# Performance work log

Hardware: AMD Instinct MI355X
Metric: run time of the kernel (lower is better)

Reference implementation:

```python
import jax, jax.numpy as jnp
import numpy as np

BN, BE, B = 50000, 800000, 16
NE, EE, GE, EH, NH = 32, 32, 32, 128, 128  # emb dims, hidden dims


def clean(x):
    return jnp.nan_to_num(x, nan=0.0, posinf=0.0, neginf=0.0)


def _lin(key, fan_in, fan_out):
    k1, k2 = jax.random.split(key)
    s = 1.0 / np.sqrt(fan_in)
    return (jax.random.uniform(k1, (fan_in, fan_out), jnp.float32, -s, s),
            jax.random.uniform(k2, (fan_out,), jnp.float32, -s, s))


def setup_inputs() -> dict:
    key = jax.random.key(0)
    ks = jax.random.split(key, 20)
    inp = {
        "x": jax.random.normal(ks[0], (BN, 2), jnp.float32),
        "edge_index": jax.random.randint(ks[1], (2, BE), 0, BN, jnp.int32),
        "batch": jax.random.randint(ks[2], (BN,), 0, B, jnp.int32),
        "node_attr": jnp.ones((BN, 2), jnp.float32),
        "edge_attr": jax.random.uniform(ks[3], (BE, 2), jnp.float32) + 0.5,  # positive spacings
        "glob_attr": jax.random.uniform(ks[4], (B, 2), jnp.float32),
    }
    # encoders (output 2*emb each, 'Duplicated')
    inp["enc_node_W"], inp["enc_node_b"] = _lin(ks[5], 2, 2 * NE)
    inp["enc_edge_W"], inp["enc_edge_b"] = _lin(ks[6], 2, 2 * EE)
    inp["enc_glob_W"], inp["enc_glob_b"] = _lin(ks[7], 2, 2 * GE)
    inp["enc2_W"], inp["enc2_b"] = _lin(ks[8], 2, 2 * EE)
    # derivative MLP: 4*NE+2*EE -> EH -> 2*EE
    inp["dW1"], inp["db1"] = _lin(ks[9], 4 * NE + 2 * EE, EH)
    inp["dW2"], inp["db2"] = _lin(ks[10], EH, 2 * EE)
    # half-jacobian MLP: 4*EE -> EH -> 2*EE
    inp["hW1"], inp["hb1"] = _lin(ks[11], 4 * EE, EH)
    inp["hW2"], inp["hb2"] = _lin(ks[12], EH, 2 * EE)
    # jacobian MLP: 6*EE -> NH -> 2*NE
    inp["jW1"], inp["jb1"] = _lin(ks[13], 6 * EE, NH)
    inp["jW2"], inp["jb2"] = _lin(ks[14], NH, 2 * NE)
    # hessian MLP: 4*EE+2*EE -> NH -> 2*NE
    inp["sW1"], inp["sb1"] = _lin(ks[15], 6 * EE, NH)
    inp["sW2"], inp["sb2"] = _lin(ks[16], NH, 2 * NE)
    # node MLP: 6*NE+2*GE -> NH -> 2*NE
    inp["nW1"], inp["nb1"] = _lin(ks[17], 6 * NE + 2 * GE, NH)
    inp["nW2"], inp["nb2"] = _lin(ks[18], NH, 2 * NE)
    # decoder: 2*NE -> 2
    inp["decW"], inp["decb"] = _lin(ks[19], 2 * NE, 2)
    return inp


def reference(x, edge_index, batch, node_attr, edge_attr, glob_attr,
              enc_node_W, enc_node_b, enc_edge_W, enc_edge_b, enc_glob_W, enc_glob_b,
              enc2_W, enc2_b,
              dW1, db1, dW2, db2,
              hW1, hb1, hW2, hb2,
              jW1, jb1, jW2, jb2,
              sW1, sb1, sW2, sb2,
              nW1, nb1, nW2, nb2,
              decW, decb):
    relu = jax.nn.relu
    seg = lambda d, idx: jax.ops.segment_sum(d, idx, num_segments=BN)
    mlp = lambda t, W1, b1, W2, b2: relu(t @ W1 + b1) @ W2 + b2

    row, col = edge_index[0], edge_index[1]
    spacing = edge_attr                                 # [BE,2]
    inv_spacing = clean(1.0 / spacing)
    inv_double = clean(1.0 / (seg(spacing, row) + seg(spacing, col)))  # [BN,2]

    node_emb = relu(x @ enc_node_W + enc_node_b)        # [BN,2*NE]
    spacing_emb = relu(spacing @ enc_edge_W + enc_edge_b)  # [BE,2*EE]
    glob_emb = relu(glob_attr @ enc_glob_W + enc_glob_b)   # [B,2*GE]
    inv_spacing_emb = relu(inv_spacing @ enc2_W + enc2_b)  # [BE,2*EE]
    inv_double_emb = relu(inv_double @ enc2_W + enc2_b)    # [BN,2*EE]

    d_edge = mlp(jnp.concatenate([node_emb[row], node_emb[col], inv_spacing_emb], -1),
                 dW1, db1, dW2, db2)                    # [BE,2*EE]
    hj_plus = seg(d_edge, row)                          # [BN,2*EE]
    hj_minus = seg(d_edge, col)

    jac1 = seg(mlp(jnp.concatenate([spacing_emb, hj_plus[col]], -1), hW1, hb1, hW2, hb2), col)
    jac2 = seg(mlp(jnp.concatenate([spacing_emb, hj_minus[row]], -1), hW1, hb1, hW2, hb2), row)
    jac = mlp(jnp.concatenate([jac1, jac2, inv_double_emb], -1), jW1, jb1, jW2, jb2)  # [BN,2*NE]

    hess = mlp(jnp.concatenate([hj_plus, hj_minus, inv_double_emb], -1), sW1, sb1, sW2, sb2)

    res = mlp(jnp.concatenate([node_emb, jac, glob_emb[batch], hess], -1), nW1, nb1, nW2, nb2)
    return node_attr * (res @ decW + decb)              # [BN,2]
```

## Files before the change

### kernel.cpp

```cpp
#include <hip/hip_runtime.h>
#include <math.h>

#define BN 50000
#define BE 800000

__device__ __forceinline__ float relu_f(float v) { return fmaxf(v, 0.0f); }
__device__ __forceinline__ float inv_clean(float s) {
    float q = 1.0f / s;
    return isfinite(q) ? q : 0.0f;
}
__device__ __forceinline__ float inv_clean_fast(float s) {
    float q = __builtin_amdgcn_rcpf(s);
    return isfinite(q) ? q : 0.0f;
}

__global__ __launch_bounds__(256) void k_pack_w1(
    const float* __restrict__ W, int r0, float4* __restrict__ dst)
{
    int t = blockIdx.x * 256 + threadIdx.x;
    if (t >= 2048) return;
    int j2 = t >> 6, l = t & 63;
    const float* ra = W + (size_t)(r0 + 2*j2) * 128 + 2*l;
    const float* rb = W + (size_t)(r0 + 2*j2 + 1) * 128 + 2*l;
    dst[t] = make_float4(ra[0], ra[1], rb[0], rb[1]);
}
__global__ __launch_bounds__(256) void k_pack_w2(
    const float* __restrict__ W2, float4* __restrict__ dst)
{
    int t = blockIdx.x * 256 + threadIdx.x;
    if (t >= 2048) return;
    int k4 = t >> 6, l = t & 63;
    dst[t] = make_float4(W2[(4*k4+0)*64+l], W2[(4*k4+1)*64+l],
                         W2[(4*k4+2)*64+l], W2[(4*k4+3)*64+l]);
}
__global__ __launch_bounds__(256) void k_pack_uv(
    const float* __restrict__ dW1, float4* __restrict__ dst)
{
    int t = blockIdx.x * 256 + threadIdx.x;
    if (t >= 4096) return;
    int j = t >> 6, l = t & 63;
    float4 w;
    if (l < 32) w = ((const float4*)(dW1 + (size_t)j*128))[l];
    else        w = ((const float4*)(dW1 + (size_t)(64+j)*128))[l-32];
    dst[t] = w;
}

__global__ __launch_bounds__(256) void k_node_enc(
    const float* __restrict__ x, const float* __restrict__ W,
    const float* __restrict__ b, float* __restrict__ node_emb)
{
    int t = blockIdx.x * 256 + threadIdx.x;
    int i = t >> 6, l = t & 63;
    float v = fmaf(x[i*2], W[l], fmaf(x[i*2+1], W[64+l], b[l]));
    node_emb[t] = relu_f(v);
}


__global__ __launch_bounds__(256, 6) void k_uv(
    const float* __restrict__ ne, const float4* __restrict__ guv,
    float* __restrict__ u, float* __restrict__ v)
{
    extern __shared__ float lds[];
    const int wid = threadIdx.x >> 6, l = threadIdx.x & 63;
    float4* xb4 = (float4*)(lds + wid * 512);
    const int gw = blockIdx.x * 4 + wid;
    const int nw = gridDim.x * 4;

    for (int g = gw; g < BN/8; g += nw) {
        const int n0 = g * 8;
        const int q = l >> 5;
        #pragma unroll
        for (int r = 0; r < 2; r++) {
            int j = (l & 31) + 32*r;
            float v0 = ne[(n0 + q*4 + 0)*64 + j];
            float v1 = ne[(n0 + q*4 + 1)*64 + j];
            float v2 = ne[(n0 + q*4 + 2)*64 + j];
            float v3 = ne[(n0 + q*4 + 3)*64 + j];
            xb4[j*2 + q] = make_float4(v0, v1, v2, v3);
        }
        float4 acc[8];
        #pragma unroll
        for (int e = 0; e < 8; e++) acc[e] = make_float4(0,0,0,0);
        #pragma unroll 8
        for (int j = 0; j < 64; j++) {
            float4 wq = guv[j*64 + l];
            float4 xa = xb4[j*2 + 0];
            float4 xc = xb4[j*2 + 1];
            acc[0].x = fmaf(xa.x, wq.x, acc[0].x); acc[0].y = fmaf(xa.x, wq.y, acc[0].y);
            acc[0].z = fmaf(xa.x, wq.z, acc[0].z); acc[0].w = fmaf(xa.x, wq.w, acc[0].w);
            acc[1].x = fmaf(xa.y, wq.x, acc[1].x); acc[1].y = fmaf(xa.y, wq.y, acc[1].y);
            acc[1].z = fmaf(xa.y, wq.z, acc[1].z); acc[1].w = fmaf(xa.y, wq.w, acc[1].w);
            acc[2].x = fmaf(xa.z, wq.x, acc[2].x); acc[2].y = fmaf(xa.z, wq.y, acc[2].y);
            acc[2].z = fmaf(xa.z, wq.z, acc[2].z); acc[2].w = fmaf(xa.z, wq.w, acc[2].w);
            acc[3].x = fmaf(xa.w, wq.x, acc[3].x); acc[3].y = fmaf(xa.w, wq.y, acc[3].y);
            acc[3].z = fmaf(xa.w, wq.z, acc[3].z); acc[3].w = fmaf(xa.w, wq.w, acc[3].w);
            acc[4].x = fmaf(xc.x, wq.x, acc[4].x); acc[4].y = fmaf(xc.x, wq.y, acc[4].y);
            acc[4].z = fmaf(xc.x, wq.z, acc[4].z); acc[4].w = fmaf(xc.x, wq.w, acc[4].w);
            acc[5].x = fmaf(xc.y, wq.x, acc[5].x); acc[5].y = fmaf(xc.y, wq.y, acc[5].y);
            acc[5].z = fmaf(xc.y, wq.z, acc[5].z); acc[5].w = fmaf(xc.y, wq.w, acc[5].w);
            acc[6].x = fmaf(xc.z, wq.x, acc[6].x); acc[6].y = fmaf(xc.z, wq.y, acc[6].y);
            acc[6].z = fmaf(xc.z, wq.z, acc[6].z); acc[6].w = fmaf(xc.z, wq.w, acc[6].w);
            acc[7].x = fmaf(xc.w, wq.x, acc[7].x); acc[7].y = fmaf(xc.w, wq.y, acc[7].y);
            acc[7].z = fmaf(xc.w, wq.z, acc[7].z); acc[7].w = fmaf(xc.w, wq.w, acc[7].w);
        }
        float* dst = (l < 32) ? (u + 4*l) : (v + 4*(l-32));
        #pragma unroll
        for (int e = 0; e < 8; e++) {
            *(float4*)(dst + (size_t)(n0+e)*128) = acc[e];
        }
    }
}

__global__ __launch_bounds__(256, 6) void k_tptm(
    const float* __restrict__ hjp, const float* __restrict__ hjm,
    const float4* __restrict__ gtp,
    float* __restrict__ tp, float* __restrict__ tm)
{
    extern __shared__ float lds[];
    const int wid = threadIdx.x >> 6, l = threadIdx.x & 63;
    float4* xb4 = (float4*)(lds + wid * 512);
    const int gw = blockIdx.x * 4 + wid;
    const int nw = gridDim.x * 4;
    const int NG = BN/8;

    for (int vg = gw; vg < 2*NG; vg += nw) {
        const float* in  = (vg < NG) ? hjp : hjm;
        float*       out = (vg < NG) ? tp  : tm;
        const int n0 = ((vg < NG) ? vg : vg - NG) * 8;
        const int q = l >> 5;
        #pragma unroll
        for (int r = 0; r < 2; r++) {
            int j = (l & 31) + 32*r;
            float v0 = in[(n0 + q*4 + 0)*64 + j];
            float v1 = in[(n0 + q*4 + 1)*64 + j];
            float v2 = in[(n0 + q*4 + 2)*64 + j];
            float v3 = in[(n0 + q*4 + 3)*64 + j];
            xb4[j*2 + q] = make_float4(v0, v1, v2, v3);
        }
        float a0[8] = {0,0,0,0,0,0,0,0}, a1[8] = {0,0,0,0,0,0,0,0};
        #pragma unroll 8
        for (int j2 = 0; j2 < 32; j2++) {
            float4 wq = gtp[j2*64 + l];
            float4 xa = xb4[(2*j2)*2 + 0];
            float4 xbv = xb4[(2*j2)*2 + 1];
            float4 xc = xb4[(2*j2+1)*2 + 0];
            float4 xd = xb4[(2*j2+1)*2 + 1];
            a0[0] = fmaf(xa.x, wq.x, fmaf(xc.x, wq.z, a0[0]));
            a1[0] = fmaf(xa.x, wq.y, fmaf(xc.x, wq.w, a1[0]));
            a0[1] = fmaf(xa.y, wq.x, fmaf(xc.y, wq.z, a0[1]));
            a1[1] = fmaf(xa.y, wq.y, fmaf(xc.y, wq.w, a1[1]));
            a0[2] = fmaf(xa.z, wq.x, fmaf(xc.z, wq.z, a0[2]));
            a1[2] = fmaf(xa.z, wq.y, fmaf(xc.z, wq.w, a1[2]));
            a0[3] = fmaf(xa.w, wq.x, fmaf(xc.w, wq.z, a0[3]));
            a1[3] = fmaf(xa.w, wq.y, fmaf(xc.w, wq.w, a1[3]));
            a0[4] = fmaf(xbv.x, wq.x, fmaf(xd.x, wq.z, a0[4]));
            a1[4] = fmaf(xbv.x, wq.y, fmaf(xd.x, wq.w, a1[4]));
            a0[5] = fmaf(xbv.y, wq.x, fmaf(xd.y, wq.z, a0[5]));
            a1[5] = fmaf(xbv.y, wq.y, fmaf(xd.y, wq.w, a1[5]));
            a0[6] = fmaf(xbv.z, wq.x, fmaf(xd.z, wq.z, a0[6]));
            a1[6] = fmaf(xbv.z, wq.y, fmaf(xd.z, wq.w, a1[6]));
            a0[7] = fmaf(xbv.w, wq.x, fmaf(xd.w, wq.z, a0[7]));
            a1[7] = fmaf(xbv.w, wq.y, fmaf(xd.w, wq.w, a1[7]));
        }
        #pragma unroll
        for (int e = 0; e < 8; e++) {
            *(float2*)(out + (size_t)(n0+e)*128 + 2*l) = make_float2(a0[e], a1[e]);
        }
    }
}

__global__ __launch_bounds__(256, 6) void k_edge1f(
    const int* __restrict__ ei, const float* __restrict__ ea,
    const float* __restrict__ u, const float* __restrict__ v,
    const float* __restrict__ e2w, const float* __restrict__ e2b,
    const float4* __restrict__ gw1, const float* __restrict__ db1,
    const float4* __restrict__ gw2, const float* __restrict__ db2,
    float* __restrict__ sumsp, float* __restrict__ hjp, float* __restrict__ hjm)
{
    extern __shared__ float lds[];
    const int wid = threadIdx.x >> 6, l = threadIdx.x & 63;
    float* buf = lds + wid * 1024;
    float4* buf4 = (float4*)buf;

    const int jA = l >> 1;
    const int eh = l & 1;
    const float ewA0 = e2w[jA],      ewB0 = e2w[64+jA],    eb0v = e2b[jA];
    const float ewA1 = e2w[jA+32],   ewB1 = e2w[96+jA],    eb1v = e2b[jA+32];
    const float b1a = db1[2*l], b1b = db1[2*l+1];
    const float b2r = db2[l];

    const int gw = blockIdx.x * 4 + wid;
    const int nw = gridDim.x * 4;

    for (int g = gw; g < BE/8; g += nw) {
        const int e0 = g * 8;
        int4 r01 = *(const int4*)(ei + e0);
        int4 r2  = *(const int4*)(ei + e0 + 4);
        int4 c01 = *(const int4*)(ei + BE + e0);
        int4 c2  = *(const int4*)(ei + BE + e0 + 4);
        float4 sv0 = ((const float4*)(ea + 2*e0))[0];
        float4 sv1 = ((const float4*)(ea + 2*e0))[1];
        float4 sv2 = ((const float4*)(ea + 2*e0))[2];
        float4 sv3 = ((const float4*)(ea + 2*e0))[3];

        if (l < 32) {
            int e = l >> 2, wch = l & 3;
            int4 rA = (e & 4) ? r2 : r01;
            int rx = (e & 2) ? ((e & 1) ? rA.w : rA.z) : ((e & 1) ? rA.y : rA.x);
            int4 cA = (e & 4) ? c2 : c01;
            int cx = (e & 2) ? ((e & 1) ? cA.w : cA.z) : ((e & 1) ? cA.y : cA.x);
            float4 sA = (e & 4) ? ((e & 2) ? sv3 : sv2) : ((e & 2) ? sv1 : sv0);
            float s0e = (e & 1) ? sA.z : sA.x;
            float s1e = (e & 1) ? sA.w : sA.y;
            int node = (wch < 2) ? rx : cx;
            int comp = wch & 1;
            float val = comp ? s1e : s0e;
            atomicAdd(&sumsp[node*2 + comp], val);
        }

        {
            float4 svA = eh ? sv2 : sv0;
            float4 svB = eh ? sv3 : sv1;
            float q00 = inv_clean_fast(svA.x), q10 = inv_clean_fast(svA.y);
            float q01 = inv_clean_fast(svA.z), q11 = inv_clean_fast(svA.w);
            float q02 = inv_clean_fast(svB.x), q12 = inv_clean_fast(svB.y);
            float q03 = inv_clean_fast(svB.z), q13 = inv_clean_fast(svB.w);
            float4 p0, p1;
            p0.x = relu_f(fmaf(q00, ewA0, fmaf(q10, ewB0, eb0v)));
            p0.y = relu_f(fmaf(q01, ewA0, fmaf(q11, ewB0, eb0v)));
            p0.z = relu_f(fmaf(q02, ewA0, fmaf(q12, ewB0, eb0v)));
            p0.w = relu_f(fmaf(q03, ewA0, fmaf(q13, ewB0, eb0v)));
            p1.x = relu_f(fmaf(q00, ewA1, fmaf(q10, ewB1, eb1v)));
            p1.y = relu_f(fmaf(q01, ewA1, fmaf(q11, ewB1, eb1v)));
            p1.z = relu_f(fmaf(q02, ewA1, fmaf(q12, ewB1, eb1v)));
            p1.w = relu_f(fmaf(q03, ewA1, fmaf(q13, ewB1, eb1v)));
            buf4[jA*2 + eh]      = p0;
            buf4[(jA+32)*2 + eh] = p1;
        }

        float t0[8], t1[8];
        {
            const int rr[8] = {r01.x, r01.y, r01.z, r01.w, r2.x, r2.y, r2.z, r2.w};
            const int cc[8] = {c01.x, c01.y, c01.z, c01.w, c2.x, c2.y, c2.z, c2.w};
            #pragma unroll
            for (int e = 0; e < 8; e++) {
                float2 uu = *(const float2*)(u + (size_t)rr[e]*128 + 2*l);
                float2 vv = *(const float2*)(v + (size_t)cc[e]*128 + 2*l);
                t0[e] = b1a + uu.x + vv.x;
                t1[e] = b1b + uu.y + vv.y;
            }
        }

        #pragma unroll 8
        for (int j2 = 0; j2 < 32; j2++) {
            float4 wq = gw1[j2*64 + l];
            float4 xa = buf4[(2*j2)*2 + 0];
            float4 xbv = buf4[(2*j2)*2 + 1];
            float4 xc = buf4[(2*j2+1)*2 + 0];
            float4 xd = buf4[(2*j2+1)*2 + 1];
            t0[0] = fmaf(xa.x, wq.x, fmaf(xc.x, wq.z, t0[0]));
            t1[0] = fmaf(xa.x, wq.y, fmaf(xc.x, wq.w, t1[0]));
            t0[1] = fmaf(xa.y, wq.x, fmaf(xc.y, wq.z, t0[1]));
            t1[1] = fmaf(xa.y, wq.y, fmaf(xc.y, wq.w, t1[1]));
            t0[2] = fmaf(xa.z, wq.x, fmaf(xc.z, wq.z, t0[2]));
            t1[2] = fmaf(xa.z, wq.y, fmaf(xc.z, wq.w, t1[2]));
            t0[3] = fmaf(xa.w, wq.x, fmaf(xc.w, wq.z, t0[3]));
            t1[3] = fmaf(xa.w, wq.y, fmaf(xc.w, wq.w, t1[3]));
            t0[4] = fmaf(xbv.x, wq.x, fmaf(xd.x, wq.z, t0[4]));
            t1[4] = fmaf(xbv.x, wq.y, fmaf(xd.x, wq.w, t1[4]));
            t0[5] = fmaf(xbv.y, wq.x, fmaf(xd.y, wq.z, t0[5]));
            t1[5] = fmaf(xbv.y, wq.y, fmaf(xd.y, wq.w, t1[5]));
            t0[6] = fmaf(xbv.z, wq.x, fmaf(xd.z, wq.z, t0[6]));
            t1[6] = fmaf(xbv.z, wq.y, fmaf(xd.z, wq.w, t1[6]));
            t0[7] = fmaf(xbv.w, wq.x, fmaf(xd.w, wq.z, t0[7]));
            t1[7] = fmaf(xbv.w, wq.y, fmaf(xd.w, wq.w, t1[7]));
        }

        #pragma unroll
        for (int e = 0; e < 8; e++) {
            *(float2*)(buf + e*128 + 2*l) = make_float2(relu_f(t0[e]), relu_f(t1[e]));
        }
        float o[8] = {0,0,0,0,0,0,0,0};
        #pragma unroll 8
        for (int k4 = 0; k4 < 32; k4++) {
            float4 wq = gw2[k4*64 + l];
            #pragma unroll
            for (int e = 0; e < 8; e++) {
                float4 hb = *(const float4*)(buf + e*128 + 4*k4);
                o[e] = fmaf(hb.x, wq.x, fmaf(hb.y, wq.y,
                        fmaf(hb.z, wq.z, fmaf(hb.w, wq.w, o[e]))));
            }
        }
        {
            const int rr[8] = {r01.x, r01.y, r01.z, r01.w, r2.x, r2.y, r2.z, r2.w};
            const int cc[8] = {c01.x, c01.y, c01.z, c01.w, c2.x, c2.y, c2.z, c2.w};
            #pragma unroll
            for (int e = 0; e < 8; e++) {
                float ov = o[e] + b2r;
                atomicAdd(&hjp[(size_t)rr[e]*64 + l], ov);
                atomicAdd(&hjm[(size_t)cc[e]*64 + l], ov);
            }
        }
    }
}

__global__ __launch_bounds__(256, 6) void k_edge2f(
    const int* __restrict__ ei, const float* __restrict__ ea,
    const float* __restrict__ tp, const float* __restrict__ tm,
    const float* __restrict__ eew, const float* __restrict__ eeb,
    const float4* __restrict__ gw1, const float* __restrict__ hb1,
    const float4* __restrict__ gw2, const float* __restrict__ hb2,
    float* __restrict__ jac1, float* __restrict__ jac2)
{
    extern __shared__ float lds[];
    const int wid = threadIdx.x >> 6, l = threadIdx.x & 63;
    float* buf = lds + wid * 1024;
    float4* buf4 = (float4*)buf;

    const int jA = l >> 1;
    const int eh = l & 1;
    const float ewA0 = eew[jA],    ewB0 = eew[64+jA],  eb0v = eeb[jA];
    const float ewA1 = eew[jA+32], ewB1 = eew[96+jA],  eb1v = eeb[jA+32];
    const float b1a = hb1[2*l], b1b = hb1[2*l+1];
    const float b2r = hb2[l];

    const int gw = blockIdx.x * 4 + wid;
    const int nw = gridDim.x * 4;

    for (int g = gw; g < BE/8; g += nw) {
        const int e0 = g * 8;
        int4 r01 = *(const int4*)(ei + e0);
        int4 r2  = *(const int4*)(ei + e0 + 4);
        int4 c01 = *(const int4*)(ei + BE + e0);
        int4 c2  = *(const int4*)(ei + BE + e0 + 4);
        float4 sv0 = ((const float4*)(ea + 2*e0))[0];
        float4 sv1 = ((const float4*)(ea + 2*e0))[1];
        float4 sv2 = ((const float4*)(ea + 2*e0))[2];
        float4 sv3 = ((const float4*)(ea + 2*e0))[3];

        {
            float4 svA = eh ? sv2 : sv0;
            float4 svB = eh ? sv3 : sv1;
            float4 p0, p1;
            p0.x = relu_f(fmaf(svA.x, ewA0, fmaf(svA.y, ewB0, eb0v)));
            p0.y = relu_f(fmaf(svA.z, ewA0, fmaf(svA.w, ewB0, eb0v)));
            p0.z = relu_f(fmaf(svB.x, ewA0, fmaf(svB.y, ewB0, eb0v)));
            p0.w = relu_f(fmaf(svB.z, ewA0, fmaf(svB.w, ewB0, eb0v)));
            p1.x = relu_f(fmaf(svA.x, ewA1, fmaf(svA.y, ewB1, eb1v)));
            p1.y = relu_f(fmaf(svA.z, ewA1, fmaf(svA.w, ewB1, eb1v)));
            p1.z = relu_f(fmaf(svB.x, ewA1, fmaf(svB.y, ewB1, eb1v)));
            p1.w = relu_f(fmaf(svB.z, ewA1, fmaf(svB.w, ewB1, eb1v)));
            buf4[jA*2 + eh]      = p0;
            buf4[(jA+32)*2 + eh] = p1;
        }

        const int rr[8] = {r01.x, r01.y, r01.z, r01.w, r2.x, r2.y, r2.z, r2.w};
        const int cc[8] = {c01.x, c01.y, c01.z, c01.w, c2.x, c2.y, c2.z, c2.w};

        float2 tpv[8];
        #pragma unroll
        for (int e = 0; e < 8; e++)
            tpv[e] = *(const float2*)(tp + (size_t)cc[e]*128 + 2*l);

        float t0[8], t1[8];
        #pragma unroll
        for (int e = 0; e < 8; e++) { t0[e] = b1a; t1[e] = b1b; }

        #pragma unroll 8
        for (int j2 = 0; j2 < 32; j2++) {
            float4 wq = gw1[j2*64 + l];
            float4 xa = buf4[(2*j2)*2 + 0];
            float4 xbv = buf4[(2*j2)*2 + 1];
            float4 xc = buf4[(2*j2+1)*2 + 0];
            float4 xd = buf4[(2*j2+1)*2 + 1];
            t0[0] = fmaf(xa.x, wq.x, fmaf(xc.x, wq.z, t0[0]));
            t1[0] = fmaf(xa.x, wq.y, fmaf(xc.x, wq.w, t1[0]));
            t0[1] = fmaf(xa.y, wq.x, fmaf(xc.y, wq.z, t0[1]));
            t1[1] = fmaf(xa.y, wq.y, fmaf(xc.y, wq.w, t1[1]));
            t0[2] = fmaf(xa.z, wq.x, fmaf(xc.z, wq.z, t0[2]));
            t1[2] = fmaf(xa.z, wq.y, fmaf(xc.z, wq.w, t1[2]));
            t0[3] = fmaf(xa.w, wq.x, fmaf(xc.w, wq.z, t0[3]));
            t1[3] = fmaf(xa.w, wq.y, fmaf(xc.w, wq.w, t1[3]));
            t0[4] = fmaf(xbv.x, wq.x, fmaf(xd.x, wq.z, t0[4]));
            t1[4] = fmaf(xbv.x, wq.y, fmaf(xd.x, wq.w, t1[4]));
            t0[5] = fmaf(xbv.y, wq.x, fmaf(xd.y, wq.z, t0[5]));
            t1[5] = fmaf(xbv.y, wq.y, fmaf(xd.y, wq.w, t1[5]));
            t0[6] = fmaf(xbv.z, wq.x, fmaf(xd.z, wq.z, t0[6]));
            t1[6] = fmaf(xbv.z, wq.y, fmaf(xd.z, wq.w, t1[6]));
            t0[7] = fmaf(xbv.w, wq.x, fmaf(xd.w, wq.z, t0[7]));
            t1[7] = fmaf(xbv.w, wq.y, fmaf(xd.w, wq.w, t1[7]));
        }

        #pragma unroll
        for (int e = 0; e < 8; e++) {
            *(float2*)(buf + e*128 + 2*l) =
                make_float2(relu_f(t0[e] + tpv[e].x), relu_f(t1[e] + tpv[e].y));
        }
        float2 tmv[8];
        #pragma unroll
        for (int e = 0; e < 8; e++)
            tmv[e] = *(const float2*)(tm + (size_t)rr[e]*128 + 2*l);

        float o1[8] = {0,0,0,0,0,0,0,0};
        #pragma unroll 8
        for (int k4 = 0; k4 < 32; k4++) {
            float4 wq = gw2[k4*64 + l];
            #pragma unroll
            for (int e = 0; e < 8; e++) {
                float4 hb = *(const float4*)(buf + e*128 + 4*k4);
                o1[e] = fmaf(hb.x, wq.x, fmaf(hb.y, wq.y,
                         fmaf(hb.z, wq.z, fmaf(hb.w, wq.w, o1[e]))));
            }
        }
        #pragma unroll
        for (int e = 0; e < 8; e++)
            atomicAdd(&jac1[(size_t)cc[e]*64 + l], o1[e] + b2r);

        #pragma unroll
        for (int e = 0; e < 8; e++) {
            *(float2*)(buf + e*128 + 2*l) =
                make_float2(relu_f(t0[e] + tmv[e].x), relu_f(t1[e] + tmv[e].y));
        }
        float o2[8] = {0,0,0,0,0,0,0,0};
        #pragma unroll 8
        for (int k4 = 0; k4 < 32; k4++) {
            float4 wq = gw2[k4*64 + l];
            #pragma unroll
            for (int e = 0; e < 8; e++) {
                float4 hb = *(const float4*)(buf + e*128 + 4*k4);
                o2[e] = fmaf(hb.x, wq.x, fmaf(hb.y, wq.y,
                         fmaf(hb.z, wq.z, fmaf(hb.w, wq.w, o2[e]))));
            }
        }
        #pragma unroll
        for (int e = 0; e < 8; e++)
            atomicAdd(&jac2[(size_t)rr[e]*64 + l], o2[e] + b2r);
    }
}

__global__ __launch_bounds__(256, 4) void k_node_mlp(
    const float* __restrict__ A, const float* __restrict__ Bv,
    const float* __restrict__ sumsp,
    const float* __restrict__ e2w_g, const float* __restrict__ e2b_g,
    const float* __restrict__ W1g, const float* __restrict__ b1g,
    const float* __restrict__ W2g, const float* __restrict__ b2g,
    float* __restrict__ outp)
{
    extern __shared__ float lds[];
    const int wid = threadIdx.x >> 6, l = threadIdx.x & 63;
    float* xbuf = lds + wid * 768;
    float* hbuf = lds + 4*768 + wid * 512;

    const float ewl = e2w_g[l], ewl2 = e2w_g[64+l], ebl = e2b_g[l];
    const float bb0 = b1g[2*l], bb1 = b1g[2*l+1];
    const float bo = b2g[l];

    const int gw = blockIdx.x * 4 + wid;
    const int nw = gridDim.x * 4;

    for (int g = gw; g < BN/4; g += nw) {
        const int i0 = g * 4;
        float av[4], bv[4], iv[4];
        #pragma unroll
        for (int e = 0; e < 4; e++) {
            int i = i0 + e;
            av[e] = A[i*64 + l];
            bv[e] = Bv[i*64 + l];
            float q0 = inv_clean(sumsp[i*2+0]);
            float q1 = inv_clean(sumsp[i*2+1]);
            iv[e] = relu_f(fmaf(q0, ewl, fmaf(q1, ewl2, ebl)));
        }
        ((float4*)xbuf)[l]       = make_float4(av[0], av[1], av[2], av[3]);
        ((float4*)xbuf)[64 + l]  = make_float4(bv[0], bv[1], bv[2], bv[3]);
        ((float4*)xbuf)[128 + l] = make_float4(iv[0], iv[1], iv[2], iv[3]);

        float acc0[4] = {0,0,0,0}, acc1[4] = {0,0,0,0};
        #pragma unroll 8
        for (int j = 0; j < 192; j++) {
            float4 xv = ((const float4*)xbuf)[j];
            float2 wv = ((const float2*)(W1g + j*128))[l];
            acc0[0] = fmaf(xv.x, wv.x, acc0[0]);
            acc0[1] = fmaf(xv.y, wv.x, acc0[1]);
            acc0[2] = fmaf(xv.z, wv.x, acc0[2]);
            acc0[3] = fmaf(xv.w, wv.x, acc0[3]);
            acc1[0] = fmaf(xv.x, wv.y, acc1[0]);
            acc1[1] = fmaf(xv.y, wv.y, acc1[1]);
            acc1[2] = fmaf(xv.z, wv.y, acc1[2]);
            acc1[3] = fmaf(xv.w, wv.y, acc1[3]);
        }
        #pragma unroll
        for (int e = 0; e < 4; e++) {
            ((float2*)(hbuf + e*128))[l] = make_float2(relu_f(acc0[e]+bb0), relu_f(acc1[e]+bb1));
        }
        float o[4] = {0,0,0,0};
        #pragma unroll 8
        for (int k = 0; k < 128; k++) {
            float wv = W2g[k*64 + l];
            o[0] = fmaf(hbuf[0*128+k], wv, o[0]);
            o[1] = fmaf(hbuf[1*128+k], wv, o[1]);
            o[2] = fmaf(hbuf[2*128+k], wv, o[2]);
            o[3] = fmaf(hbuf[3*128+k], wv, o[3]);
        }
        #pragma unroll
        for (int e = 0; e < 4; e++) outp[(i0+e)*64 + l] = o[e] + bo;
    }
}

__global__ __launch_bounds__(256, 4) void k_node_final(
    const float* __restrict__ node_emb, const float* __restrict__ jacv,
    const float* __restrict__ hessv,
    const int* __restrict__ batch, const float* __restrict__ ga,
    const float* __restrict__ gw_g, const float* __restrict__ gb_g,
    const float* __restrict__ nW1, const float* __restrict__ nb1,
    const float* __restrict__ nW2, const float* __restrict__ nb2,
    const float* __restrict__ decW, const float* __restrict__ decb,
    const float* __restrict__ node_attr, float* __restrict__ outp)
{
    extern __shared__ float lds[];
    const int wid = threadIdx.x >> 6, l = threadIdx.x & 63;
    float* xbuf = lds + wid * 1024;
    float* hbuf = lds + 4*1024 + wid * 512;

    const float gwl = gw_g[l], gwl2 = gw_g[64+l], gbl = gb_g[l];
    const float bb0 = nb1[2*l], bb1 = nb1[2*l+1];
    const float bo = nb2[l];

    const int gwv = blockIdx.x * 4 + wid;
    const int nw = gridDim.x * 4;

    for (int g = gwv; g < BN/4; g += nw) {
        const int i0 = g * 4;
        float ne[4], jv[4], ge[4], hv[4];
        #pragma unroll
        for (int e = 0; e < 4; e++) {
            int i = i0 + e;
            ne[e] = node_emb[i*64 + l];
            jv[e] = jacv[i*64 + l];
            hv[e] = hessv[i*64 + l];
            int gi = batch[i];
            ge[e] = relu_f(fmaf(ga[gi*2], gwl, fmaf(ga[gi*2+1], gwl2, gbl)));
        }
        ((float4*)xbuf)[l]       = make_float4(ne[0], ne[1], ne[2], ne[3]);
        ((float4*)xbuf)[64 + l]  = make_float4(jv[0], jv[1], jv[2], jv[3]);
        ((float4*)xbuf)[128 + l] = make_float4(ge[0], ge[1], ge[2], ge[3]);
        ((float4*)xbuf)[192 + l] = make_float4(hv[0], hv[1], hv[2], hv[3]);

        float acc0[4] = {0,0,0,0}, acc1[4] = {0,0,0,0};
        #pragma unroll 8
        for (int j = 0; j < 256; j++) {
            float4 xv = ((const float4*)xbuf)[j];
            float2 wv = ((const float2*)(nW1 + j*128))[l];
            acc0[0] = fmaf(xv.x, wv.x, acc0[0]);
            acc0[1] = fmaf(xv.y, wv.x, acc0[1]);
            acc0[2] = fmaf(xv.z, wv.x, acc0[2]);
            acc0[3] = fmaf(xv.w, wv.x, acc0[3]);
            acc1[0] = fmaf(xv.x, wv.y, acc1[0]);
            acc1[1] = fmaf(xv.y, wv.y, acc1[1]);
            acc1[2] = fmaf(xv.z, wv.y, acc1[2]);
            acc1[3] = fmaf(xv.w, wv.y, acc1[3]);
        }
        #pragma unroll
        for (int e = 0; e < 4; e++) {
            ((float2*)(hbuf + e*128))[l] = make_float2(relu_f(acc0[e]+bb0), relu_f(acc1[e]+bb1));
        }
        float o[4] = {0,0,0,0};
        #pragma unroll 8
        for (int k = 0; k < 128; k++) {
            float wv = nW2[k*64 + l];
            o[0] = fmaf(hbuf[0*128+k], wv, o[0]);
            o[1] = fmaf(hbuf[1*128+k], wv, o[1]);
            o[2] = fmaf(hbuf[2*128+k], wv, o[2]);
            o[3] = fmaf(hbuf[3*128+k], wv, o[3]);
        }
        #pragma unroll
        for (int e = 0; e < 4; e++) hbuf[e*128 + l] = o[e] + bo;

        int e2 = l >> 4, sub = l & 15, j2 = sub >> 3, part = sub & 7;
        float s = 0.0f;
        #pragma unroll
        for (int kk = 0; kk < 8; kk++) {
            int k = part*8 + kk;
            s = fmaf(hbuf[e2*128 + k], decW[k*2 + j2], s);
        }
        s += __shfl_xor(s, 1);
        s += __shfl_xor(s, 2);
        s += __shfl_xor(s, 4);
        if (part == 0) {
            int i = i0 + e2;
            outp[i*2 + j2] = (s + decb[j2]) * node_attr[i*2 + j2];
        }
    }
}

__global__ __launch_bounds__(256) void k_edge1(
    const int* __restrict__ ei, const float* __restrict__ ea,
    const float* __restrict__ node_emb,
    const float* __restrict__ e2w_g, const float* __restrict__ e2b_g,
    const float* __restrict__ dW1, const float* __restrict__ db1,
    const float* __restrict__ dW2, const float* __restrict__ db2,
    float* __restrict__ sumsp, float* __restrict__ hjp, float* __restrict__ hjm)
{
    extern __shared__ float lds[];
    float* w1 = lds;
    float* b1 = w1 + 192*128;
    float* w2 = b1 + 128;
    float* b2 = w2 + 128*64;
    float* ew = b2 + 64;
    float* eb = ew + 128;
    float* xreg = eb + 64;
    float* hreg = xreg + 4*768;

    for (int idx = threadIdx.x; idx < 192*128; idx += 256) w1[idx] = dW1[idx];
    for (int idx = threadIdx.x; idx < 128*64; idx += 256)  w2[idx] = dW2[idx];
    if (threadIdx.x < 128) { b1[threadIdx.x] = db1[threadIdx.x]; ew[threadIdx.x] = e2w_g[threadIdx.x]; }
    if (threadIdx.x < 64)  { b2[threadIdx.x] = db2[threadIdx.x]; eb[threadIdx.x] = e2b_g[threadIdx.x]; }
    __syncthreads();

    const int wid = threadIdx.x >> 6, l = threadIdx.x & 63;
    float* xbuf = xreg + wid * 768;
    float* hbuf = hreg + wid * 512;
    const int gw = blockIdx.x * 4 + wid;
    const int nw = gridDim.x * 4;

    for (int g = gw; g < BE/4; g += nw) {
        const int e0 = g * 4;
        int r[4], c[4];
        float s0[4], s1[4];
        #pragma unroll
        for (int e = 0; e < 4; e++) {
            r[e]  = ei[e0+e];
            c[e]  = ei[BE + e0+e];
            s0[e] = ea[(e0+e)*2+0];
            s1[e] = ea[(e0+e)*2+1];
        }
        if (l < 16) {
            int e = l >> 2, wch = l & 3;
            int node = (wch < 2) ? r[e] : c[e];
            float v = (wch & 1) ? s1[e] : s0[e];
            atomicAdd(&sumsp[node*2 + (wch & 1)], v);
        }
        float ar[4], cr[4], ir[4];
        #pragma unroll
        for (int e = 0; e < 4; e++) {
            ar[e] = node_emb[r[e]*64 + l];
            cr[e] = node_emb[c[e]*64 + l];
            float q0 = inv_clean(s0[e]), q1 = inv_clean(s1[e]);
            ir[e] = relu_f(fmaf(q0, ew[l], fmaf(q1, ew[64+l], eb[l])));
        }
        ((float4*)xbuf)[l]       = make_float4(ar[0], ar[1], ar[2], ar[3]);
        ((float4*)xbuf)[64 + l]  = make_float4(cr[0], cr[1], cr[2], cr[3]);
        ((float4*)xbuf)[128 + l] = make_float4(ir[0], ir[1], ir[2], ir[3]);

        float acc0[4] = {0,0,0,0}, acc1[4] = {0,0,0,0};
        #pragma unroll 8
        for (int j = 0; j < 192; j++) {
            float4 xv = ((const float4*)xbuf)[j];
            float2 wv = ((const float2*)(w1 + j*128))[l];
            acc0[0] = fmaf(xv.x, wv.x, acc0[0]);
            acc0[1] = fmaf(xv.y, wv.x, acc0[1]);
            acc0[2] = fmaf(xv.z, wv.x, acc0[2]);
            acc0[3] = fmaf(xv.w, wv.x, acc0[3]);
            acc1[0] = fmaf(xv.x, wv.y, acc1[0]);
            acc1[1] = fmaf(xv.y, wv.y, acc1[1]);
            acc1[2] = fmaf(xv.z, wv.y, acc1[2]);
            acc1[3] = fmaf(xv.w, wv.y, acc1[3]);
        }
        float bb0 = b1[2*l], bb1 = b1[2*l+1];
        #pragma unroll
        for (int e = 0; e < 4; e++) {
            float2 h = make_float2(relu_f(acc0[e]+bb0), relu_f(acc1[e]+bb1));
            ((float2*)(hbuf + e*128))[l] = h;
        }
        float o[4] = {0,0,0,0};
        #pragma unroll 8
        for (int k = 0; k < 128; k++) {
            float wv = w2[k*64 + l];
            o[0] = fmaf(hbuf[0*128+k], wv, o[0]);
            o[1] = fmaf(hbuf[1*128+k], wv, o[1]);
            o[2] = fmaf(hbuf[2*128+k], wv, o[2]);
            o[3] = fmaf(hbuf[3*128+k], wv, o[3]);
        }
        float bo = b2[l];
        #pragma unroll
        for (int e = 0; e < 4; e++) {
            float ov = o[e] + bo;
            atomicAdd(&hjp[r[e]*64 + l], ov);
            atomicAdd(&hjm[c[e]*64 + l], ov);
        }
    }
}

__global__ __launch_bounds__(256) void k_edge2(
    const int* __restrict__ ei, const float* __restrict__ ea,
    const float* __restrict__ hjp, const float* __restrict__ hjm,
    const float* __restrict__ eew_g, const float* __restrict__ eeb_g,
    const float* __restrict__ hW1, const float* __restrict__ hb1,
    const float* __restrict__ hW2, const float* __restrict__ hb2,
    float* __restrict__ jac1, float* __restrict__ jac2)
{
    extern __shared__ float lds[];
    float* w1 = lds;
    float* b1 = w1 + 128*128;
    float* w2 = b1 + 128;
    float* b2 = w2 + 128*64;
    float* ew = b2 + 64;
    float* eb = ew + 128;
    float* base = eb + 64;

    for (int idx = threadIdx.x; idx < 128*128; idx += 256) w1[idx] = hW1[idx];
    for (int idx = threadIdx.x; idx < 128*64; idx += 256)  w2[idx] = hW2[idx];
    if (threadIdx.x < 128) { b1[threadIdx.x] = hb1[threadIdx.x]; ew[threadIdx.x] = eew_g[threadIdx.x]; }
    if (threadIdx.x < 64)  { b2[threadIdx.x] = hb2[threadIdx.x]; eb[threadIdx.x] = eeb_g[threadIdx.x]; }
    __syncthreads();

    const int wid = threadIdx.x >> 6, l = threadIdx.x & 63;
    float* x1 = base + wid*2048;
    float* x2 = x1 + 512;
    float* h1 = x2 + 512;
    float* h2 = h1 + 512;
    const int gw = blockIdx.x * 4 + wid;
    const int nw = gridDim.x * 4;

    for (int g = gw; g < BE/4; g += nw) {
        const int e0 = g * 4;
        int r[4], c[4];
        float se[4], pa[4], pb[4];
        #pragma unroll
        for (int e = 0; e < 4; e++) {
            r[e] = ei[e0+e];
            c[e] = ei[BE + e0+e];
            float sp0 = ea[(e0+e)*2+0], sp1 = ea[(e0+e)*2+1];
            se[e] = relu_f(fmaf(sp0, ew[l], fmaf(sp1, ew[64+l], eb[l])));
            pa[e] = hjp[c[e]*64 + l];
            pb[e] = hjm[r[e]*64 + l];
        }
        ((float4*)x1)[l]      = make_float4(se[0], se[1], se[2], se[3]);
        ((float4*)x1)[64 + l] = make_float4(pa[0], pa[1], pa[2], pa[3]);
        ((float4*)x2)[l]      = make_float4(se[0], se[1], se[2], se[3]);
        ((float4*)x2)[64 + l] = make_float4(pb[0], pb[1], pb[2], pb[3]);

        float a0[4]={0,0,0,0}, a1[4]={0,0,0,0}, b0v[4]={0,0,0,0}, b1v[4]={0,0,0,0};
        #pragma unroll 8
        for (int j = 0; j < 128; j++) {
            float2 wv = ((const float2*)(w1 + j*128))[l];
            float4 xa = ((const float4*)x1)[j];
            float4 xb = ((const float4*)x2)[j];
            a0[0]=fmaf(xa.x,wv.x,a0[0]); a0[1]=fmaf(xa.y,wv.x,a0[1]);
            a0[2]=fmaf(xa.z,wv.x,a0[2]); a0[3]=fmaf(xa.w,wv.x,a0[3]);
            a1[0]=fmaf(xa.x,wv.y,a1[0]); a1[1]=fmaf(xa.y,wv.y,a1[1]);
            a1[2]=fmaf(xa.z,wv.y,a1[2]); a1[3]=fmaf(xa.w,wv.y,a1[3]);
            b0v[0]=fmaf(xb.x,wv.x,b0v[0]); b0v[1]=fmaf(xb.y,wv.x,b0v[1]);
            b0v[2]=fmaf(xb.z,wv.x,b0v[2]); b0v[3]=fmaf(xb.w,wv.x,b0v[3]);
            b1v[0]=fmaf(xb.x,wv.y,b1v[0]); b1v[1]=fmaf(xb.y,wv.y,b1v[1]);
            b1v[2]=fmaf(xb.z,wv.y,b1v[2]); b1v[3]=fmaf(xb.w,wv.y,b1v[3]);
        }
        float bb0 = b1[2*l], bb1 = b1[2*l+1];
        #pragma unroll
        for (int e = 0; e < 4; e++) {
            ((float2*)(h1 + e*128))[l] = make_float2(relu_f(a0[e]+bb0), relu_f(a1[e]+bb1));
            ((float2*)(h2 + e*128))[l] = make_float2(relu_f(b0v[e]+bb0), relu_f(b1v[e]+bb1));
        }
        float oA[4]={0,0,0,0}, oB[4]={0,0,0,0};
        #pragma unroll 8
        for (int k = 0; k < 128; k++) {
            float wv = w2[k*64 + l];
            oA[0]=fmaf(h1[0*128+k],wv,oA[0]); oA[1]=fmaf(h1[1*128+k],wv,oA[1]);
            oA[2]=fmaf(h1[2*128+k],wv,oA[2]); oA[3]=fmaf(h1[3*128+k],wv,oA[3]);
            oB[0]=fmaf(h2[0*128+k],wv,oB[0]); oB[1]=fmaf(h2[1*128+k],wv,oB[1]);
            oB[2]=fmaf(h2[2*128+k],wv,oB[2]); oB[3]=fmaf(h2[3*128+k],wv,oB[3]);
        }
        float bo = b2[l];
        #pragma unroll
        for (int e = 0; e < 4; e++) {
            atomicAdd(&jac1[c[e]*64 + l], oA[e] + bo);
            atomicAdd(&jac2[r[e]*64 + l], oB[e] + bo);
        }
    }
}

extern "C" void kernel_launch(void* const* d_in, const int* in_sizes, int n_in,
                              void* d_out, int out_size, void* d_ws, size_t ws_size,
                              hipStream_t stream) {
    const float* x          = (const float*)d_in[0];
    const int*   ei         = (const int*)  d_in[1];
    const int*   batch      = (const int*)  d_in[2];
    const float* node_attr  = (const float*)d_in[3];
    const float* edge_attr  = (const float*)d_in[4];
    const float* glob_attr  = (const float*)d_in[5];
    const float* enc_node_W = (const float*)d_in[6];
    const float* enc_node_b = (const float*)d_in[7];
    const float* enc_edge_W = (const float*)d_in[8];
    const float* enc_edge_b = (const float*)d_in[9];
    const float* enc_glob_W = (const float*)d_in[10];
    const float* enc_glob_b = (const float*)d_in[11];
    const float* enc2_W     = (const float*)d_in[12];
    const float* enc2_b     = (const float*)d_in[13];
    const float* dW1 = (const float*)d_in[14]; const float* db1 = (const float*)d_in[15];
    const float* dW2 = (const float*)d_in[16]; const float* db2 = (const float*)d_in[17];
    const float* hW1 = (const float*)d_in[18]; const float* hb1 = (const float*)d_in[19];
    const float* hW2 = (const float*)d_in[20]; const float* hb2 = (const float*)d_in[21];
    const float* jW1 = (const float*)d_in[22]; const float* jb1 = (const float*)d_in[23];
    const float* jW2 = (const float*)d_in[24]; const float* jb2 = (const float*)d_in[25];
    const float* sW1 = (const float*)d_in[26]; const float* sb1 = (const float*)d_in[27];
    const float* sW2 = (const float*)d_in[28]; const float* sb2 = (const float*)d_in[29];
    const float* nW1 = (const float*)d_in[30]; const float* nb1 = (const float*)d_in[31];
    const float* nW2 = (const float*)d_in[32]; const float* nb2 = (const float*)d_in[33];
    const float* decW = (const float*)d_in[34]; const float* decb = (const float*)d_in[35];

    float* ws = (float*)d_ws;
    const size_t NEED_FAST = 28900000ull * sizeof(float);

    if (ws_size >= NEED_FAST) {
        float* ne    = ws;
        float* u     = ne + 3200000;
        float* v     = u + 6400000;
        float* hjp   = v + 6400000;
        float* hjm   = hjp + 3200000;
        float* jac1  = hjm + 3200000;
        float* jac2  = jac1 + 3200000;
        float* sumsp = jac2 + 3200000;

        float* scratch = (float*)d_out;
        float4* puv   = (float4*)(scratch);
        float4* pw1e1 = (float4*)(scratch + 16384);
        float4* pw2e1 = (float4*)(scratch + 24576);
        float4* pw1tp = (float4*)(scratch + 32768);
        float4* pw1e2 = (float4*)(scratch + 40960);
        float4* pw2e2 = (float4*)(scratch + 49152);

        hipMemsetAsync(hjp, 0, (size_t)4*3200000*sizeof(float), stream);
        hipMemsetAsync(sumsp, 0, (size_t)100000*sizeof(float), stream);

        k_pack_uv<<<16, 256, 0, stream>>>(dW1, puv);
        k_pack_w1<<<8, 256, 0, stream>>>(dW1, 128, pw1e1);
        k_pack_w2<<<8, 256, 0, stream>>>(dW2, pw2e1);
        k_pack_w1<<<8, 256, 0, stream>>>(hW1, 64, pw1tp);
        k_pack_w1<<<8, 256, 0, stream>>>(hW1, 0, pw1e2);
        k_pack_w2<<<8, 256, 0, stream>>>(hW2, pw2e2);

        k_node_enc<<<12500, 256, 0, stream>>>(x, enc_node_W, enc_node_b, ne);

        k_uv<<<1536, 256, 2048*4, stream>>>(ne, puv, u, v);

        k_edge1f<<<1536, 256, 4096*4, stream>>>(ei, edge_attr, u, v, enc2_W, enc2_b,
                                                pw1e1, db1, pw2e1, db2, sumsp, hjp, hjm);

        k_tptm<<<1536, 256, 2048*4, stream>>>(hjp, hjm, pw1tp, u, v);

        k_edge2f<<<1536, 256, 4096*4, stream>>>(ei, edge_attr, u, v,
                                                enc_edge_W, enc_edge_b,
                                                pw1e2, hb1, pw2e2, hb2, jac1, jac2);

        size_t lds_nm = (4*768 + 4*512) * sizeof(float);
        k_node_mlp<<<1024, 256, lds_nm, stream>>>(jac1, jac2, sumsp, enc2_W, enc2_b,
                                                  jW1, jb1, jW2, jb2, jac1);
        k_node_mlp<<<1024, 256, lds_nm, stream>>>(hjp, hjm, sumsp, enc2_W, enc2_b,
                                                  sW1, sb1, sW2, sb2, hjp);

        size_t lds_nf = (4*1024 + 4*512) * sizeof(float);
        k_node_final<<<1024, 256, lds_nf, stream>>>(ne, jac1, hjp,
                                                    batch, glob_attr, enc_glob_W, enc_glob_b,
                                                    nW1, nb1, nW2, nb2, decW, decb,
                                                    node_attr, (float*)d_out);
    } else {
        float* node_emb = ws;
        float* hjp   = node_emb + 3200000;
        float* hjm   = hjp + 3200000;
        float* jac1  = hjm + 3200000;
        float* jac2  = jac1 + 3200000;
        float* sumsp = jac2 + 3200000;

        hipMemsetAsync(hjp, 0, (size_t)4*3200000*sizeof(float), stream);
        hipMemsetAsync(sumsp, 0, (size_t)100000*sizeof(float), stream);

        k_node_enc<<<12500, 256, 0, stream>>>(x, enc_node_W, enc_node_b, node_emb);

        size_t lds1 = 38272u * sizeof(float);
        k_edge1<<<256, 256, lds1, stream>>>(ei, edge_attr, node_emb, enc2_W, enc2_b,
                                            dW1, db1, dW2, db2, sumsp, hjp, hjm);

        size_t lds2 = 33152u * sizeof(float);
        k_edge2<<<256, 256, lds2, stream>>>(ei, edge_attr, hjp, hjm,
                                            enc_edge_W, enc_edge_b,
                                            hW1, hb1, hW2, hb2, jac1, jac2);

        size_t lds_nm = (4*768 + 4*512) * sizeof(float);
        k_node_mlp<<<1024, 256, lds_nm, stream>>>(jac1, jac2, sumsp, enc2_W, enc2_b,
                                                  jW1, jb1, jW2, jb2, jac1);
        k_node_mlp<<<1024, 256, lds_nm, stream>>>(hjp, hjm, sumsp, enc2_W, enc2_b,
                                                  sW1, sb1, sW2, sb2, hjp);

        size_t lds_nf = (4*1024 + 4*512) * sizeof(float);
        k_node_final<<<1024, 256, lds_nf, stream>>>(node_emb, jac1, hjp,
                                                    batch, glob_attr, enc_glob_W, enc_glob_b,
                                                    nW1, nb1, nW2, nb2, decW, decb,
                                                    node_attr, (float*)d_out);
    }
}
```

Measured before the change: 2.092 ms.

## Sort edges by destination via CSR and merge atomics per run

Builds CSR-style sorted edge lists for rows and columns on the device (histogram, scan, scatter), then reruns the edge MLP kernels once per direction over the sorted lists. Consecutive edges that share a destination are accumulated in registers and flushed with a single atomic, which replaces per-edge atomics and the atomic segment sum of spacings. It also recomputes node embeddings inside the final kernel, because the node-embedding buffer is reused for the CSR arrays. The cost is running the edge-1 MLP twice (once per direction) plus the gather overhead of indirect edge ids.

```diff
diff --git a/kernel.cpp b/kernel.cpp
--- a/kernel.cpp
+++ b/kernel.cpp
@@ -3,6 +3,7 @@
 
 #define BN 50000
 #define BE 800000
+#define CHUNK 200
 
 __device__ __forceinline__ float relu_f(float v) { return fmaxf(v, 0.0f); }
 __device__ __forceinline__ float inv_clean(float s) {
@@ -45,6 +46,77 @@
     dst[t] = w;
 }
 
+__global__ __launch_bounds__(256) void k_hist(
+    const int* __restrict__ ei, int* __restrict__ rc, int* __restrict__ cc)
+{
+    int e = blockIdx.x * 256 + threadIdx.x;
+    if (e >= BE) return;
+    atomicAdd(&rc[ei[e]], 1);
+    atomicAdd(&cc[ei[BE + e]], 1);
+}
+
+__global__ __launch_bounds__(1024) void k_scan(
+    const int* __restrict__ cntR, int* __restrict__ offR, int* __restrict__ hdR,
+    const int* __restrict__ cntC, int* __restrict__ offC, int* __restrict__ hdC)
+{
+    __shared__ int s[1024];
+    const int* cnt; int* off; int* hd;
+    if (blockIdx.x == 0) { cnt = cntR; off = offR; hd = hdR; }
+    else                 { cnt = cntC; off = offC; hd = hdC; }
+    int t = threadIdx.x;
+    int base = t * 49;
+    int sum = 0;
+    for (int i = 0; i < 49; i++) {
+        int idx = base + i;
+        sum += (idx < BN) ? cnt[idx] : 0;
+    }
+    s[t] = sum;
+    __syncthreads();
+    for (int o = 1; o < 1024; o <<= 1) {
+        int v = (t >= o) ? s[t - o] : 0;
+        __syncthreads();
+        s[t] += v;
+        __syncthreads();
+    }
+    int run = s[t] - sum;
+    for (int i = 0; i < 49; i++) {
+        int idx = base + i;
+        if (idx < BN) {
+            off[idx] = run;
+            hd[idx] = run;
+            run += cnt[idx];
+        }
+    }
+    if (t == 1023) off[BN] = run;
+}
+
+__global__ __launch_bounds__(256) void k_scatter(
+    const int* __restrict__ ei, int* __restrict__ rhd, int* __restrict__ chd,
+    int* __restrict__ rel, int* __restrict__ cel)
+{
+    int e = blockIdx.x * 256 + threadIdx.x;
+    if (e >= BE) return;
+    int p1 = atomicAdd(&rhd[ei[e]], 1);      rel[p1] = e;
+    int p2 = atomicAdd(&chd[ei[BE + e]], 1); cel[p2] = e;
+}
+
+__global__ __launch_bounds__(256) void k_sumsp(
+    const float* __restrict__ ea,
+    const int* __restrict__ roff, const int* __restrict__ rel,
+    const int* __restrict__ coff, const int* __restrict__ cel,
+    float* __restrict__ sumsp)
+{
+    int n = blockIdx.x * 256 + threadIdx.x;
+    if (n >= BN) return;
+    float s0 = 0.f, s1 = 0.f;
+    int e0 = roff[n], e1 = roff[n+1];
+    for (int j = e0; j < e1; j++) { int e = rel[j]; s0 += ea[2*e]; s1 += ea[2*e+1]; }
+    e0 = coff[n]; e1 = coff[n+1];
+    for (int j = e0; j < e1; j++) { int e = cel[j]; s0 += ea[2*e]; s1 += ea[2*e+1]; }
+    sumsp[2*n]   = s0;
+    sumsp[2*n+1] = s1;
+}
+
 __global__ __launch_bounds__(256) void k_node_enc(
     const float* __restrict__ x, const float* __restrict__ W,
     const float* __restrict__ b, float* __restrict__ node_emb)
@@ -54,7 +126,6 @@
     float v = fmaf(x[i*2], W[l], fmaf(x[i*2+1], W[64+l], b[l]));
     node_emb[t] = relu_f(v);
 }
-
 
 __global__ __launch_bounds__(256, 6) void k_uv(
     const float* __restrict__ ne, const float4* __restrict__ guv,
@@ -169,13 +240,14 @@
     }
 }
 
-__global__ __launch_bounds__(256, 6) void k_edge1f(
-    const int* __restrict__ ei, const float* __restrict__ ea,
+__global__ __launch_bounds__(256, 6) void k_edge1s(
+    const int* __restrict__ elist, const int* __restrict__ ei,
+    const float* __restrict__ ea,
     const float* __restrict__ u, const float* __restrict__ v,
     const float* __restrict__ e2w, const float* __restrict__ e2b,
     const float4* __restrict__ gw1, const float* __restrict__ db1,
     const float4* __restrict__ gw2, const float* __restrict__ db2,
-    float* __restrict__ sumsp, float* __restrict__ hjp, float* __restrict__ hjm)
+    int mergeRow, float* __restrict__ out)
 {
     extern __shared__ float lds[];
     const int wid = threadIdx.x >> 6, l = threadIdx.x & 63;
@@ -189,66 +261,57 @@
     const float b1a = db1[2*l], b1b = db1[2*l+1];
     const float b2r = db2[l];
 
-    const int gw = blockIdx.x * 4 + wid;
-    const int nw = gridDim.x * 4;
-
-    for (int g = gw; g < BE/8; g += nw) {
-        const int e0 = g * 8;
-        int4 r01 = *(const int4*)(ei + e0);
-        int4 r2  = *(const int4*)(ei + e0 + 4);
-        int4 c01 = *(const int4*)(ei + BE + e0);
-        int4 c2  = *(const int4*)(ei + BE + e0 + 4);
-        float4 sv0 = ((const float4*)(ea + 2*e0))[0];
-        float4 sv1 = ((const float4*)(ea + 2*e0))[1];
-        float4 sv2 = ((const float4*)(ea + 2*e0))[2];
-        float4 sv3 = ((const float4*)(ea + 2*e0))[3];
-
-        if (l < 32) {
-            int e = l >> 2, wch = l & 3;
-            int4 rA = (e & 4) ? r2 : r01;
-            int rx = (e & 2) ? ((e & 1) ? rA.w : rA.z) : ((e & 1) ? rA.y : rA.x);
-            int4 cA = (e & 4) ? c2 : c01;
-            int cx = (e & 2) ? ((e & 1) ? cA.w : cA.z) : ((e & 1) ? cA.y : cA.x);
-            float4 sA = (e & 4) ? ((e & 2) ? sv3 : sv2) : ((e & 2) ? sv1 : sv0);
-            float s0e = (e & 1) ? sA.z : sA.x;
-            float s1e = (e & 1) ? sA.w : sA.y;
-            int node = (wch < 2) ? rx : cx;
-            int comp = wch & 1;
-            float val = comp ? s1e : s0e;
-            atomicAdd(&sumsp[node*2 + comp], val);
-        }
-
+    const int wave = blockIdx.x * 4 + wid;
+    const int start = wave * CHUNK;
+    const int end = min(start + CHUNK, BE);
+
+    float acc = 0.f;
+    int cur = -1;
+
+    for (int i = start; i < end; i += 8) {
+        const int nact = min(8, end - i);
+        int eid[8], rr[8], cc[8];
+        float2 spv[8];
+        #pragma unroll
+        for (int e = 0; e < 8; e++) {
+            int idx = i + ((e < nact) ? e : nact - 1);
+            eid[e] = elist[idx];
+        }
+        #pragma unroll
+        for (int e = 0; e < 8; e++) {
+            rr[e] = ei[eid[e]];
+            cc[e] = ei[BE + eid[e]];
+            spv[e] = *(const float2*)(ea + 2*(size_t)eid[e]);
+        }
         {
-            float4 svA = eh ? sv2 : sv0;
-            float4 svB = eh ? sv3 : sv1;
-            float q00 = inv_clean_fast(svA.x), q10 = inv_clean_fast(svA.y);
-            float q01 = inv_clean_fast(svA.z), q11 = inv_clean_fast(svA.w);
-            float q02 = inv_clean_fast(svB.x), q12 = inv_clean_fast(svB.y);
-            float q03 = inv_clean_fast(svB.z), q13 = inv_clean_fast(svB.w);
+            float2 sA = eh ? spv[4] : spv[0];
+            float2 sB = eh ? spv[5] : spv[1];
+            float2 sC = eh ? spv[6] : spv[2];
+            float2 sD = eh ? spv[7] : spv[3];
+            float qA0 = inv_clean_fast(sA.x), qA1 = inv_clean_fast(sA.y);
+            float qB0 = inv_clean_fast(sB.x), qB1 = inv_clean_fast(sB.y);
+            float qC0 = inv_clean_fast(sC.x), qC1 = inv_clean_fast(sC.y);
+            float qD0 = inv_clean_fast(sD.x), qD1 = inv_clean_fast(sD.y);
             float4 p0, p1;
-            p0.x = relu_f(fmaf(q00, ewA0, fmaf(q10, ewB0, eb0v)));
-            p0.y = relu_f(fmaf(q01, ewA0, fmaf(q11, ewB0, eb0v)));
-            p0.z = relu_f(fmaf(q02, ewA0, fmaf(q12, ewB0, eb0v)));
-            p0.w = relu_f(fmaf(q03, ewA0, fmaf(q13, ewB0, eb0v)));
-            p1.x = relu_f(fmaf(q00, ewA1, fmaf(q10, ewB1, eb1v)));
-            p1.y = relu_f(fmaf(q01, ewA1, fmaf(q11, ewB1, eb1v)));
-            p1.z = relu_f(fmaf(q02, ewA1, fmaf(q12, ewB1, eb1v)));
-            p1.w = relu_f(fmaf(q03, ewA1, fmaf(q13, ewB1, eb1v)));
+            p0.x = relu_f(fmaf(qA0, ewA0, fmaf(qA1, ewB0, eb0v)));
+            p0.y = relu_f(fmaf(qB0, ewA0, fmaf(qB1, ewB0, eb0v)));
+            p0.z = relu_f(fmaf(qC0, ewA0, fmaf(qC1, ewB0, eb0v)));
+            p0.w = relu_f(fmaf(qD0, ewA0, fmaf(qD1, ewB0, eb0v)));
+            p1.x = relu_f(fmaf(qA0, ewA1, fmaf(qA1, ewB1, eb1v)));
+            p1.y = relu_f(fmaf(qB0, ewA1, fmaf(qB1, ewB1, eb1v)));
+            p1.z = relu_f(fmaf(qC0, ewA1, fmaf(qC1, ewB1, eb1v)));
+            p1.w = relu_f(fmaf(qD0, ewA1, fmaf(qD1, ewB1, eb1v)));
             buf4[jA*2 + eh]      = p0;
             buf4[(jA+32)*2 + eh] = p1;
         }
 
         float t0[8], t1[8];
-        {
-            const int rr[8] = {r01.x, r01.y, r01.z, r01.w, r2.x, r2.y, r2.z, r2.w};
-            const int cc[8] = {c01.x, c01.y, c01.z, c01.w, c2.x, c2.y, c2.z, c2.w};
-            #pragma unroll
-            for (int e = 0; e < 8; e++) {
-                float2 uu = *(const float2*)(u + (size_t)rr[e]*128 + 2*l);
-                float2 vv = *(const float2*)(v + (size_t)cc[e]*128 + 2*l);
-                t0[e] = b1a + uu.x + vv.x;
-                t1[e] = b1b + uu.y + vv.y;
-            }
+        #pragma unroll
+        for (int e = 0; e < 8; e++) {
+            float2 uu = *(const float2*)(u + (size_t)rr[e]*128 + 2*l);
+            float2 vv = *(const float2*)(v + (size_t)cc[e]*128 + 2*l);
+            t0[e] = b1a + uu.x + vv.x;
+            t1[e] = b1b + uu.y + vv.y;
         }
 
         #pragma unroll 8
@@ -291,26 +354,30 @@
                         fmaf(hb.z, wq.z, fmaf(hb.w, wq.w, o[e]))));
             }
         }
-        {
-            const int rr[8] = {r01.x, r01.y, r01.z, r01.w, r2.x, r2.y, r2.z, r2.w};
-            const int cc[8] = {c01.x, c01.y, c01.z, c01.w, c2.x, c2.y, c2.z, c2.w};
-            #pragma unroll
-            for (int e = 0; e < 8; e++) {
-                float ov = o[e] + b2r;
-                atomicAdd(&hjp[(size_t)rr[e]*64 + l], ov);
-                atomicAdd(&hjm[(size_t)cc[e]*64 + l], ov);
+        #pragma unroll
+        for (int e = 0; e < 8; e++) {
+            if (e < nact) {
+                int k = mergeRow ? rr[e] : cc[e];
+                float val = o[e] + b2r;
+                if (k != cur) {
+                    if (cur >= 0) atomicAdd(&out[(size_t)cur*64 + l], acc);
+                    acc = 0.f;
+                    cur = k;
+                }
+                acc += val;
             }
         }
     }
-}
-
-__global__ __launch_bounds__(256, 6) void k_edge2f(
-    const int* __restrict__ ei, const float* __restrict__ ea,
-    const float* __restrict__ tp, const float* __restrict__ tm,
+    if (cur >= 0) atomicAdd(&out[(size_t)cur*64 + l], acc);
+}
+
+__global__ __launch_bounds__(256, 6) void k_edge2s(
+    const int* __restrict__ elist, const int* __restrict__ ei,
+    const float* __restrict__ ea, const float* __restrict__ tvals,
     const float* __restrict__ eew, const float* __restrict__ eeb,
     const float4* __restrict__ gw1, const float* __restrict__ hb1,
     const float4* __restrict__ gw2, const float* __restrict__ hb2,
-    float* __restrict__ jac1, float* __restrict__ jac2)
+    int mergeRow, float* __restrict__ out)
 {
     extern __shared__ float lds[];
     const int wid = threadIdx.x >> 6, l = threadIdx.x & 63;
@@ -324,43 +391,49 @@
     const float b1a = hb1[2*l], b1b = hb1[2*l+1];
     const float b2r = hb2[l];
 
-    const int gw = blockIdx.x * 4 + wid;
-    const int nw = gridDim.x * 4;
-
-    for (int g = gw; g < BE/8; g += nw) {
-        const int e0 = g * 8;
-        int4 r01 = *(const int4*)(ei + e0);
-        int4 r2  = *(const int4*)(ei + e0 + 4);
-        int4 c01 = *(const int4*)(ei + BE + e0);
-        int4 c2  = *(const int4*)(ei + BE + e0 + 4);
-        float4 sv0 = ((const float4*)(ea + 2*e0))[0];
-        float4 sv1 = ((const float4*)(ea + 2*e0))[1];
-        float4 sv2 = ((const float4*)(ea + 2*e0))[2];
-        float4 sv3 = ((const float4*)(ea + 2*e0))[3];
-
+    const int wave = blockIdx.x * 4 + wid;
+    const int start = wave * CHUNK;
+    const int end = min(start + CHUNK, BE);
+
+    float acc = 0.f;
+    int cur = -1;
+
+    for (int i = start; i < end; i += 8) {
+        const int nact = min(8, end - i);
+        int eid[8], kk[8];
+        float2 spv[8];
+        #pragma unroll
+        for (int e = 0; e < 8; e++) {
+            int idx = i + ((e < nact) ? e : nact - 1);
+            eid[e] = elist[idx];
+        }
+        #pragma unroll
+        for (int e = 0; e < 8; e++) {
+            kk[e] = mergeRow ? ei[eid[e]] : ei[BE + eid[e]];
+            spv[e] = *(const float2*)(ea + 2*(size_t)eid[e]);
+        }
         {
-            float4 svA = eh ? sv2 : sv0;
-            float4 svB = eh ? sv3 : sv1;
+            float2 sA = eh ? spv[4] : spv[0];
+            float2 sB = eh ? spv[5] : spv[1];
+            float2 sC = eh ? spv[6] : spv[2];
+            float2 sD = eh ? spv[7] : spv[3];
             float4 p0, p1;
-            p0.x = relu_f(fmaf(svA.x, ewA0, fmaf(svA.y, ewB0, eb0v)));
-            p0.y = relu_f(fmaf(svA.z, ewA0, fmaf(svA.w, ewB0, eb0v)));
-            p0.z = relu_f(fmaf(svB.x, ewA0, fmaf(svB.y, ewB0, eb0v)));
-            p0.w = relu_f(fmaf(svB.z, ewA0, fmaf(svB.w, ewB0, eb0v)));
-            p1.x = relu_f(fmaf(svA.x, ewA1, fmaf(svA.y, ewB1, eb1v)));
-            p1.y = relu_f(fmaf(svA.z, ewA1, fmaf(svA.w, ewB1, eb1v)));
-            p1.z = relu_f(fmaf(svB.x, ewA1, fmaf(svB.y, ewB1, eb1v)));
-            p1.w = relu_f(fmaf(svB.z, ewA1, fmaf(svB.w, ewB1, eb1v)));
+            p0.x = relu_f(fmaf(sA.x, ewA0, fmaf(sA.y, ewB0, eb0v)));
+            p0.y = relu_f(fmaf(sB.x, ewA0, fmaf(sB.y, ewB0, eb0v)));
+            p0.z = relu_f(fmaf(sC.x, ewA0, fmaf(sC.y, ewB0, eb0v)));
+            p0.w = relu_f(fmaf(sD.x, ewA0, fmaf(sD.y, ewB0, eb0v)));
+            p1.x = relu_f(fmaf(sA.x, ewA1, fmaf(sA.y, ewB1, eb1v)));
+            p1.y = relu_f(fmaf(sB.x, ewA1, fmaf(sB.y, ewB1, eb1v)));
+            p1.z = relu_f(fmaf(sC.x, ewA1, fmaf(sC.y, ewB1, eb1v)));
+            p1.w = relu_f(fmaf(sD.x, ewA1, fmaf(sD.y, ewB1, eb1v)));
             buf4[jA*2 + eh]      = p0;
             buf4[(jA+32)*2 + eh] = p1;
         }
 
-        const int rr[8] = {r01.x, r01.y, r01.z, r01.w, r2.x, r2.y, r2.z, r2.w};
-        const int cc[8] = {c01.x, c01.y, c01.z, c01.w, c2.x, c2.y, c2.z, c2.w};
-
-        float2 tpv[8];
+        float2 tv[8];
         #pragma unroll
         for (int e = 0; e < 8; e++)
-            tpv[e] = *(const float2*)(tp + (size_t)cc[e]*128 + 2*l);
+            tv[e] = *(const float2*)(tvals + (size_t)kk[e]*128 + 2*l);
 
         float t0[8], t1[8];
         #pragma unroll
@@ -394,48 +467,33 @@
         #pragma unroll
         for (int e = 0; e < 8; e++) {
             *(float2*)(buf + e*128 + 2*l) =
-                make_float2(relu_f(t0[e] + tpv[e].x), relu_f(t1[e] + tpv[e].y));
-        }
-        float2 tmv[8];
-        #pragma unroll
-        for (int e = 0; e < 8; e++)
-            tmv[e] = *(const float2*)(tm + (size_t)rr[e]*128 + 2*l);
-
-        float o1[8] = {0,0,0,0,0,0,0,0};
+                make_float2(relu_f(t0[e] + tv[e].x), relu_f(t1[e] + tv[e].y));
+        }
+        float o[8] = {0,0,0,0,0,0,0,0};
         #pragma unroll 8
         for (int k4 = 0; k4 < 32; k4++) {
             float4 wq = gw2[k4*64 + l];
             #pragma unroll
             for (int e = 0; e < 8; e++) {
                 float4 hb = *(const float4*)(buf + e*128 + 4*k4);
-                o1[e] = fmaf(hb.x, wq.x, fmaf(hb.y, wq.y,
-                         fmaf(hb.z, wq.z, fmaf(hb.w, wq.w, o1[e]))));
+                o[e] = fmaf(hb.x, wq.x, fmaf(hb.y, wq.y,
+                         fmaf(hb.z, wq.z, fmaf(hb.w, wq.w, o[e]))));
             }
         }
         #pragma unroll
-        for (int e = 0; e < 8; e++)
-            atomicAdd(&jac1[(size_t)cc[e]*64 + l], o1[e] + b2r);
-
-        #pragma unroll
-        for (int e = 0; e < 8; e++) {
-            *(float2*)(buf + e*128 + 2*l) =
-                make_float2(relu_f(t0[e] + tmv[e].x), relu_f(t1[e] + tmv[e].y));
-        }
-        float o2[8] = {0,0,0,0,0,0,0,0};
-        #pragma unroll 8
-        for (int k4 = 0; k4 < 32; k4++) {
-            float4 wq = gw2[k4*64 + l];
-            #pragma unroll
-            for (int e = 0; e < 8; e++) {
-                float4 hb = *(const float4*)(buf + e*128 + 4*k4);
-                o2[e] = fmaf(hb.x, wq.x, fmaf(hb.y, wq.y,
-                         fmaf(hb.z, wq.z, fmaf(hb.w, wq.w, o2[e]))));
+        for (int e = 0; e < 8; e++) {
+            if (e < nact) {
+                float val = o[e] + b2r;
+                if (kk[e] != cur) {
+                    if (cur >= 0) atomicAdd(&out[(size_t)cur*64 + l], acc);
+                    acc = 0.f;
+                    cur = kk[e];
+                }
+                acc += val;
             }
         }
-        #pragma unroll
-        for (int e = 0; e < 8; e++)
-            atomicAdd(&jac2[(size_t)rr[e]*64 + l], o2[e] + b2r);
-    }
+    }
+    if (cur >= 0) atomicAdd(&out[(size_t)cur*64 + l], acc);
 }
 
 __global__ __launch_bounds__(256, 4) void k_node_mlp(
@@ -507,8 +565,9 @@
 }
 
 __global__ __launch_bounds__(256, 4) void k_node_final(
-    const float* __restrict__ node_emb, const float* __restrict__ jacv,
-    const float* __restrict__ hessv,
+    const float* __restrict__ x,
+    const float* __restrict__ enW, const float* __restrict__ enB,
+    const float* __restrict__ jacv, const float* __restrict__ hessv,
     const int* __restrict__ batch, const float* __restrict__ ga,
     const float* __restrict__ gw_g, const float* __restrict__ gb_g,
     const float* __restrict__ nW1, const float* __restrict__ nb1,
@@ -522,6 +581,7 @@
     float* hbuf = lds + 4*1024 + wid * 512;
 
     const float gwl = gw_g[l], gwl2 = gw_g[64+l], gbl = gb_g[l];
+    const float enw0 = enW[l], enw1 = enW[64+l], enb = enB[l];
     const float bb0 = nb1[2*l], bb1 = nb1[2*l+1];
     const float bo = nb2[l];
 
@@ -534,7 +594,7 @@
         #pragma unroll
         for (int e = 0; e < 4; e++) {
             int i = i0 + e;
-            ne[e] = node_emb[i*64 + l];
+            ne[e] = relu_f(fmaf(x[i*2], enw0, fmaf(x[i*2+1], enw1, enb)));
             jv[e] = jacv[i*64 + l];
             hv[e] = hessv[i*64 + l];
             int gi = batch[i];
@@ -588,192 +648,6 @@
         if (part == 0) {
             int i = i0 + e2;
             outp[i*2 + j2] = (s + decb[j2]) * node_attr[i*2 + j2];
-        }
-    }
-}
-
-__global__ __launch_bounds__(256) void k_edge1(
-    const int* __restrict__ ei, const float* __restrict__ ea,
-    const float* __restrict__ node_emb,
-    const float* __restrict__ e2w_g, const float* __restrict__ e2b_g,
-    const float* __restrict__ dW1, const float* __restrict__ db1,
-    const float* __restrict__ dW2, const float* __restrict__ db2,
-    float* __restrict__ sumsp, float* __restrict__ hjp, float* __restrict__ hjm)
-{
-    extern __shared__ float lds[];
-    float* w1 = lds;
-    float* b1 = w1 + 192*128;
-    float* w2 = b1 + 128;
-    float* b2 = w2 + 128*64;
-    float* ew = b2 + 64;
-    float* eb = ew + 128;
-    float* xreg = eb + 64;
-    float* hreg = xreg + 4*768;
-
-    for (int idx = threadIdx.x; idx < 192*128; idx += 256) w1[idx] = dW1[idx];
-    for (int idx = threadIdx.x; idx < 128*64; idx += 256)  w2[idx] = dW2[idx];
-    if (threadIdx.x < 128) { b1[threadIdx.x] = db1[threadIdx.x]; ew[threadIdx.x] = e2w_g[threadIdx.x]; }
-    if (threadIdx.x < 64)  { b2[threadIdx.x] = db2[threadIdx.x]; eb[threadIdx.x] = e2b_g[threadIdx.x]; }
-    __syncthreads();
-
-    const int wid = threadIdx.x >> 6, l = threadIdx.x & 63;
-    float* xbuf = xreg + wid * 768;
-    float* hbuf = hreg + wid * 512;
-    const int gw = blockIdx.x * 4 + wid;
-    const int nw = gridDim.x * 4;
-
-    for (int g = gw; g < BE/4; g += nw) {
-        const int e0 = g * 4;
-        int r[4], c[4];
-        float s0[4], s1[4];
-        #pragma unroll
-        for (int e = 0; e < 4; e++) {
-            r[e]  = ei[e0+e];
-            c[e]  = ei[BE + e0+e];
-            s0[e] = ea[(e0+e)*2+0];
-            s1[e] = ea[(e0+e)*2+1];
-        }
-        if (l < 16) {
-            int e = l >> 2, wch = l & 3;
-            int node = (wch < 2) ? r[e] : c[e];
-            float v = (wch & 1) ? s1[e] : s0[e];
-            atomicAdd(&sumsp[node*2 + (wch & 1)], v);
-        }
-        float ar[4], cr[4], ir[4];
-        #pragma unroll
-        for (int e = 0; e < 4; e++) {
-            ar[e] = node_emb[r[e]*64 + l];
-            cr[e] = node_emb[c[e]*64 + l];
-            float q0 = inv_clean(s0[e]), q1 = inv_clean(s1[e]);
-            ir[e] = relu_f(fmaf(q0, ew[l], fmaf(q1, ew[64+l], eb[l])));
-        }
-        ((float4*)xbuf)[l]       = make_float4(ar[0], ar[1], ar[2], ar[3]);
-        ((float4*)xbuf)[64 + l]  = make_float4(cr[0], cr[1], cr[2], cr[3]);
-        ((float4*)xbuf)[128 + l] = make_float4(ir[0], ir[1], ir[2], ir[3]);
-
-        float acc0[4] = {0,0,0,0}, acc1[4] = {0,0,0,0};
-        #pragma unroll 8
-        for (int j = 0; j < 192; j++) {
-            float4 xv = ((const float4*)xbuf)[j];
-            float2 wv = ((const float2*)(w1 + j*128))[l];
-            acc0[0] = fmaf(xv.x, wv.x, acc0[0]);
-            acc0[1] = fmaf(xv.y, wv.x, acc0[1]);
-            acc0[2] = fmaf(xv.z, wv.x, acc0[2]);
-            acc0[3] = fmaf(xv.w, wv.x, acc0[3]);
-            acc1[0] = fmaf(xv.x, wv.y, acc1[0]);
-            acc1[1] = fmaf(xv.y, wv.y, acc1[1]);
-            acc1[2] = fmaf(xv.z, wv.y, acc1[2]);
-            acc1[3] = fmaf(xv.w, wv.y, acc1[3]);
-        }
-        float bb0 = b1[2*l], bb1 = b1[2*l+1];
-        #pragma unroll
-        for (int e = 0; e < 4; e++) {
-            float2 h = make_float2(relu_f(acc0[e]+bb0), relu_f(acc1[e]+bb1));
-            ((float2*)(hbuf + e*128))[l] = h;
-        }
-        float o[4] = {0,0,0,0};
-        #pragma unroll 8
-        for (int k = 0; k < 128; k++) {
-            float wv = w2[k*64 + l];
-            o[0] = fmaf(hbuf[0*128+k], wv, o[0]);
-            o[1] = fmaf(hbuf[1*128+k], wv, o[1]);
-            o[2] = fmaf(hbuf[2*128+k], wv, o[2]);
-            o[3] = fmaf(hbuf[3*128+k], wv, o[3]);
-        }
-        float bo = b2[l];
-        #pragma unroll
-        for (int e = 0; e < 4; e++) {
-            float ov = o[e] + bo;
-            atomicAdd(&hjp[r[e]*64 + l], ov);
-            atomicAdd(&hjm[c[e]*64 + l], ov);
-        }
-    }
-}
-
-__global__ __launch_bounds__(256) void k_edge2(
-    const int* __restrict__ ei, const float* __restrict__ ea,
-    const float* __restrict__ hjp, const float* __restrict__ hjm,
-    const float* __restrict__ eew_g, const float* __restrict__ eeb_g,
-    const float* __restrict__ hW1, const float* __restrict__ hb1,
-    const float* __restrict__ hW2, const float* __restrict__ hb2,
-    float* __restrict__ jac1, float* __restrict__ jac2)
-{
-    extern __shared__ float lds[];
-    float* w1 = lds;
-    float* b1 = w1 + 128*128;
-    float* w2 = b1 + 128;
-    float* b2 = w2 + 128*64;
-    float* ew = b2 + 64;
-    float* eb = ew + 128;
-    float* base = eb + 64;
-
-    for (int idx = threadIdx.x; idx < 128*128; idx += 256) w1[idx] = hW1[idx];
-    for (int idx = threadIdx.x; idx < 128*64; idx += 256)  w2[idx] = hW2[idx];
-    if (threadIdx.x < 128) { b1[threadIdx.x] = hb1[threadIdx.x]; ew[threadIdx.x] = eew_g[threadIdx.x]; }
-    if (threadIdx.x < 64)  { b2[threadIdx.x] = hb2[threadIdx.x]; eb[threadIdx.x] = eeb_g[threadIdx.x]; }
-    __syncthreads();
-
-    const int wid = threadIdx.x >> 6, l = threadIdx.x & 63;
-    float* x1 = base + wid*2048;
-    float* x2 = x1 + 512;
-    float* h1 = x2 + 512;
-    float* h2 = h1 + 512;
-    const int gw = blockIdx.x * 4 + wid;
-    const int nw = gridDim.x * 4;
-
-    for (int g = gw; g < BE/4; g += nw) {
-        const int e0 = g * 4;
-        int r[4], c[4];
-        float se[4], pa[4], pb[4];
-        #pragma unroll
-        for (int e = 0; e < 4; e++) {
-            r[e] = ei[e0+e];
-            c[e] = ei[BE + e0+e];
-            float sp0 = ea[(e0+e)*2+0], sp1 = ea[(e0+e)*2+1];
-            se[e] = relu_f(fmaf(sp0, ew[l], fmaf(sp1, ew[64+l], eb[l])));
-            pa[e] = hjp[c[e]*64 + l];
-            pb[e] = hjm[r[e]*64 + l];
-        }
-        ((float4*)x1)[l]      = make_float4(se[0], se[1], se[2], se[3]);
-        ((float4*)x1)[64 + l] = make_float4(pa[0], pa[1], pa[2], pa[3]);
-        ((float4*)x2)[l]      = make_float4(se[0], se[1], se[2], se[3]);
-        ((float4*)x2)[64 + l] = make_float4(pb[0], pb[1], pb[2], pb[3]);
-
-        float a0[4]={0,0,0,0}, a1[4]={0,0,0,0}, b0v[4]={0,0,0,0}, b1v[4]={0,0,0,0};
-        #pragma unroll 8
-        for (int j = 0; j < 128; j++) {
-            float2 wv = ((const float2*)(w1 + j*128))[l];
-            float4 xa = ((const float4*)x1)[j];
-            float4 xb = ((const float4*)x2)[j];
-            a0[0]=fmaf(xa.x,wv.x,a0[0]); a0[1]=fmaf(xa.y,wv.x,a0[1]);
-            a0[2]=fmaf(xa.z,wv.x,a0[2]); a0[3]=fmaf(xa.w,wv.x,a0[3]);
-            a1[0]=fmaf(xa.x,wv.y,a1[0]); a1[1]=fmaf(xa.y,wv.y,a1[1]);
-            a1[2]=fmaf(xa.z,wv.y,a1[2]); a1[3]=fmaf(xa.w,wv.y,a1[3]);
-            b0v[0]=fmaf(xb.x,wv.x,b0v[0]); b0v[1]=fmaf(xb.y,wv.x,b0v[1]);
-            b0v[2]=fmaf(xb.z,wv.x,b0v[2]); b0v[3]=fmaf(xb.w,wv.x,b0v[3]);
-            b1v[0]=fmaf(xb.x,wv.y,b1v[0]); b1v[1]=fmaf(xb.y,wv.y,b1v[1]);
-            b1v[2]=fmaf(xb.z,wv.y,b1v[2]); b1v[3]=fmaf(xb.w,wv.y,b1v[3]);
-        }
-        float bb0 = b1[2*l], bb1 = b1[2*l+1];
-        #pragma unroll
-        for (int e = 0; e < 4; e++) {
-            ((float2*)(h1 + e*128))[l] = make_float2(relu_f(a0[e]+bb0), relu_f(a1[e]+bb1));
-            ((float2*)(h2 + e*128))[l] = make_float2(relu_f(b0v[e]+bb0), relu_f(b1v[e]+bb1));
-        }
-        float oA[4]={0,0,0,0}, oB[4]={0,0,0,0};
-        #pragma unroll 8
-        for (int k = 0; k < 128; k++) {
-            float wv = w2[k*64 + l];
-            oA[0]=fmaf(h1[0*128+k],wv,oA[0]); oA[1]=fmaf(h1[1*128+k],wv,oA[1]);
-            oA[2]=fmaf(h1[2*128+k],wv,oA[2]); oA[3]=fmaf(h1[3*128+k],wv,oA[3]);
-            oB[0]=fmaf(h2[0*128+k],wv,oB[0]); oB[1]=fmaf(h2[1*128+k],wv,oB[1]);
-            oB[2]=fmaf(h2[2*128+k],wv,oB[2]); oB[3]=fmaf(h2[3*128+k],wv,oB[3]);
-        }
-        float bo = b2[l];
-        #pragma unroll
-        for (int e = 0; e < 4; e++) {
-            atomicAdd(&jac1[c[e]*64 + l], oA[e] + bo);
-            atomicAdd(&jac2[r[e]*64 + l], oB[e] + bo);
         }
     }
 }
@@ -808,92 +682,75 @@
     const float* decW = (const float*)d_in[34]; const float* decb = (const float*)d_in[35];
 
     float* ws = (float*)d_ws;
-    const size_t NEED_FAST = 28900000ull * sizeof(float);
-
-    if (ws_size >= NEED_FAST) {
-        float* ne    = ws;
-        float* u     = ne + 3200000;
-        float* v     = u + 6400000;
-        float* hjp   = v + 6400000;
-        float* hjm   = hjp + 3200000;
-        float* jac1  = hjm + 3200000;
-        float* jac2  = jac1 + 3200000;
-        float* sumsp = jac2 + 3200000;
-
-        float* scratch = (float*)d_out;
-        float4* puv   = (float4*)(scratch);
-        float4* pw1e1 = (float4*)(scratch + 16384);
-        float4* pw2e1 = (float4*)(scratch + 24576);
-        float4* pw1tp = (float4*)(scratch + 32768);
-        float4* pw1e2 = (float4*)(scratch + 40960);
-        float4* pw2e2 = (float4*)(scratch + 49152);
-
-        hipMemsetAsync(hjp, 0, (size_t)4*3200000*sizeof(float), stream);
-        hipMemsetAsync(sumsp, 0, (size_t)100000*sizeof(float), stream);
-
-        k_pack_uv<<<16, 256, 0, stream>>>(dW1, puv);
-        k_pack_w1<<<8, 256, 0, stream>>>(dW1, 128, pw1e1);
-        k_pack_w2<<<8, 256, 0, stream>>>(dW2, pw2e1);
-        k_pack_w1<<<8, 256, 0, stream>>>(hW1, 64, pw1tp);
-        k_pack_w1<<<8, 256, 0, stream>>>(hW1, 0, pw1e2);
-        k_pack_w2<<<8, 256, 0, stream>>>(hW2, pw2e2);
-
-        k_node_enc<<<12500, 256, 0, stream>>>(x, enc_node_W, enc_node_b, ne);
-
-        k_uv<<<1536, 256, 2048*4, stream>>>(ne, puv, u, v);
-
-        k_edge1f<<<1536, 256, 4096*4, stream>>>(ei, edge_attr, u, v, enc2_W, enc2_b,
-                                                pw1e1, db1, pw2e1, db2, sumsp, hjp, hjm);
-
-        k_tptm<<<1536, 256, 2048*4, stream>>>(hjp, hjm, pw1tp, u, v);
-
-        k_edge2f<<<1536, 256, 4096*4, stream>>>(ei, edge_attr, u, v,
-                                                enc_edge_W, enc_edge_b,
-                                                pw1e2, hb1, pw2e2, hb2, jac1, jac2);
-
-        size_t lds_nm = (4*768 + 4*512) * sizeof(float);
-        k_node_mlp<<<1024, 256, lds_nm, stream>>>(jac1, jac2, sumsp, enc2_W, enc2_b,
-                                                  jW1, jb1, jW2, jb2, jac1);
-        k_node_mlp<<<1024, 256, lds_nm, stream>>>(hjp, hjm, sumsp, enc2_W, enc2_b,
-                                                  sW1, sb1, sW2, sb2, hjp);
-
-        size_t lds_nf = (4*1024 + 4*512) * sizeof(float);
-        k_node_final<<<1024, 256, lds_nf, stream>>>(ne, jac1, hjp,
-                                                    batch, glob_attr, enc_glob_W, enc_glob_b,
-                                                    nW1, nb1, nW2, nb2, decW, decb,
-                                                    node_attr, (float*)d_out);
-    } else {
-        float* node_emb = ws;
-        float* hjp   = node_emb + 3200000;
-        float* hjm   = hjp + 3200000;
-        float* jac1  = hjm + 3200000;
-        float* jac2  = jac1 + 3200000;
-        float* sumsp = jac2 + 3200000;
-
-        hipMemsetAsync(hjp, 0, (size_t)4*3200000*sizeof(float), stream);
-        hipMemsetAsync(sumsp, 0, (size_t)100000*sizeof(float), stream);
-
-        k_node_enc<<<12500, 256, 0, stream>>>(x, enc_node_W, enc_node_b, node_emb);
-
-        size_t lds1 = 38272u * sizeof(float);
-        k_edge1<<<256, 256, lds1, stream>>>(ei, edge_attr, node_emb, enc2_W, enc2_b,
-                                            dW1, db1, dW2, db2, sumsp, hjp, hjm);
-
-        size_t lds2 = 33152u * sizeof(float);
-        k_edge2<<<256, 256, lds2, stream>>>(ei, edge_attr, hjp, hjm,
+    float* ne    = ws;
+    float* u     = ne + 3200000;
+    float* v     = u + 6400000;
+    float* hjp   = v + 6400000;
+    float* hjm   = hjp + 3200000;
+    float* jac1  = hjm + 3200000;
+    float* jac2  = jac1 + 3200000;
+    float* sumsp = jac2 + 3200000;
+
+    int* A       = (int*)ne;
+    int* row_cnt = A;
+    int* col_cnt = A + 50176;
+    int* row_off = A + 100352;
+    int* col_off = A + 150400;
+    int* row_hd  = A + 200448;
+    int* col_hd  = A + 250496;
+    int* row_el  = A + 300544;
+    int* col_el  = A + 1100544;
+
+    float* scratch = (float*)d_out;
+    float4* puv   = (float4*)(scratch);
+    float4* pw1e1 = (float4*)(scratch + 16384);
+    float4* pw2e1 = (float4*)(scratch + 24576);
+    float4* pw1tp = (float4*)(scratch + 32768);
+    float4* pw1e2 = (float4*)(scratch + 40960);
+    float4* pw2e2 = (float4*)(scratch + 49152);
+
+    hipMemsetAsync(hjp, 0, (size_t)4*3200000*sizeof(float), stream);
+
+    k_pack_uv<<<16, 256, 0, stream>>>(dW1, puv);
+    k_pack_w1<<<8, 256, 0, stream>>>(dW1, 128, pw1e1);
+    k_pack_w2<<<8, 256, 0, stream>>>(dW2, pw2e1);
+    k_pack_w1<<<8, 256, 0, stream>>>(hW1, 64, pw1tp);
+    k_pack_w1<<<8, 256, 0, stream>>>(hW1, 0, pw1e2);
+    k_pack_w2<<<8, 256, 0, stream>>>(hW2, pw2e2);
+
+    k_node_enc<<<12500, 256, 0, stream>>>(x, enc_node_W, enc_node_b, ne);
+    k_uv<<<1536, 256, 2048*4, stream>>>(ne, puv, u, v);
+
+    hipMemsetAsync(A, 0, (size_t)100352*sizeof(int), stream);
+    k_hist<<<3125, 256, 0, stream>>>(ei, row_cnt, col_cnt);
+    k_scan<<<2, 1024, 0, stream>>>(row_cnt, row_off, row_hd, col_cnt, col_off, col_hd);
+    k_scatter<<<3125, 256, 0, stream>>>(ei, row_hd, col_hd, row_el, col_el);
+    k_sumsp<<<196, 256, 0, stream>>>(edge_attr, row_off, row_el, col_off, col_el, sumsp);
+
+    k_edge1s<<<1000, 256, 4096*4, stream>>>(row_el, ei, edge_attr, u, v, enc2_W, enc2_b,
+                                            pw1e1, db1, pw2e1, db2, 1, hjp);
+    k_edge1s<<<1000, 256, 4096*4, stream>>>(col_el, ei, edge_attr, u, v, enc2_W, enc2_b,
+                                            pw1e1, db1, pw2e1, db2, 0, hjm);
+
+    k_tptm<<<1536, 256, 2048*4, stream>>>(hjp, hjm, pw1tp, u, v);
+
+    k_edge2s<<<1000, 256, 4096*4, stream>>>(col_el, ei, edge_attr, u,
                                             enc_edge_W, enc_edge_b,
-                                            hW1, hb1, hW2, hb2, jac1, jac2);
-
-        size_t lds_nm = (4*768 + 4*512) * sizeof(float);
-        k_node_mlp<<<1024, 256, lds_nm, stream>>>(jac1, jac2, sumsp, enc2_W, enc2_b,
-                                                  jW1, jb1, jW2, jb2, jac1);
-        k_node_mlp<<<1024, 256, lds_nm, stream>>>(hjp, hjm, sumsp, enc2_W, enc2_b,
-                                                  sW1, sb1, sW2, sb2, hjp);
-
-        size_t lds_nf = (4*1024 + 4*512) * sizeof(float);
-        k_node_final<<<1024, 256, lds_nf, stream>>>(node_emb, jac1, hjp,
-                                                    batch, glob_attr, enc_glob_W, enc_glob_b,
-                                                    nW1, nb1, nW2, nb2, decW, decb,
-                                                    node_attr, (float*)d_out);
-    }
-}
+                                            pw1e2, hb1, pw2e2, hb2, 0, jac1);
+    k_edge2s<<<1000, 256, 4096*4, stream>>>(row_el, ei, edge_attr, v,
+                                            enc_edge_W, enc_edge_b,
+                                            pw1e2, hb1, pw2e2, hb2, 1, jac2);
+
+    size_t lds_nm = (4*768 + 4*512) * sizeof(float);
+    k_node_mlp<<<1024, 256, lds_nm, stream>>>(jac1, jac2, sumsp, enc2_W, enc2_b,
+                                              jW1, jb1, jW2, jb2, jac1);
+    k_node_mlp<<<1024, 256, lds_nm, stream>>>(hjp, hjm, sumsp, enc2_W, enc2_b,
+                                              sW1, sb1, sW2, sb2, hjp);
+
+    size_t lds_nf = (4*1024 + 4*512) * sizeof(float);
+    k_node_final<<<1024, 256, lds_nf, stream>>>(x, enc_node_W, enc_node_b,
+                                                jac1, hjp,
+                                                batch, glob_attr, enc_glob_W, enc_glob_b,
+                                                nW1, nb1, nW2, nb2, decW, decb,
+                                                node_attr, (float*)d_out);
+}
```

Result: slower. 3.724 ms (+78.0%).
